# Optimization experiments

Measured on AMD Instinct MI355X. Metric: run time of the kernel, lower is better.

Reference implementation:

```python
import jax, jax.numpy as jnp
import numpy as np

C_S = 384; C_Z = 128; C_RES = 128; H = 12; HD = 32; L = 8; RB = 2; NA = 7
TSF = 10.0; EPS = 1e-8; B = 2; N = 512; NRES = 21


def layernorm(x, g, b, eps=1e-5):
    m = jnp.mean(x, -1, keepdims=True)
    v = jnp.mean((x - m) ** 2, -1, keepdims=True)
    return (x - m) * jax.lax.rsqrt(v + eps) * g + b


def lin(x, w, b=None):
    y = x @ w.T
    return y if b is None else y + b


def rot_vec(R, v):
    return jnp.einsum('...ij,...j->...i', R, v)


def make_rigid(n, ca, c, eps=1e-7):
    # Gram-Schmidt backbone frame construction (openfold make_transform_from_reference)
    t = -ca
    n_xyz = n + t; c_xyz = c + t
    cx, cy, cz = c_xyz[..., 0], c_xyz[..., 1], c_xyz[..., 2]
    z = jnp.zeros_like(cx); o = jnp.ones_like(cx)
    nrm = jnp.sqrt(eps + cx**2 + cy**2)
    s1 = -cy / nrm; c1 = cx / nrm
    R1 = jnp.stack([jnp.stack([c1, -s1, z], -1), jnp.stack([s1, c1, z], -1), jnp.stack([z, z, o], -1)], -2)
    nrm2 = jnp.sqrt(eps + cx**2 + cy**2 + cz**2)
    s2 = cz / nrm2; c2 = jnp.sqrt(cx**2 + cy**2) / nrm2
    R2 = jnp.stack([jnp.stack([c2, z, s2], -1), jnp.stack([z, o, z], -1), jnp.stack([-s2, z, c2], -1)], -2)
    Rc = R2 @ R1
    n2 = rot_vec(Rc, n_xyz)
    ny, nz = n2[..., 1], n2[..., 2]
    nrm3 = jnp.sqrt(eps + ny**2 + nz**2)
    sn = -nz / nrm3; cn = ny / nrm3
    Rn = jnp.stack([jnp.stack([o, z, z], -1), jnp.stack([z, cn, -sn], -1), jnp.stack([z, sn, cn], -1)], -2)
    R = jnp.swapaxes(Rn @ Rc, -1, -2)
    return R, ca


def to4x4(R, t):
    bot = jnp.zeros(R.shape[:-2] + (1, 4), R.dtype).at[..., 0, 3].set(1.0)
    top = jnp.concatenate([R, t[..., None]], -1)
    return jnp.concatenate([top, bot], -2)


def compose(R1, t1, R2, t2):
    return R1 @ R2, rot_vec(R1, t2) + t1


def structure_fwd(s, z, aatype, mask, ln_s_g, ln_s_b, ln_z_g, ln_z_b, w_in, b_in, w_b, b_b,
                  attn_ln_g, attn_ln_b, attn_wqkv, attn_wo, attn_bo, attn_wg, attn_bg,
                  tr_ln_g, tr_ln_b, tr_w1, tr_b1, tr_w2, tr_b2, w_bb, b_bb,
                  ar_win, ar_bin, ar_winit, ar_binit, ar_w1, ar_b1, ar_w2, ar_b2, ar_wout, ar_bout,
                  default_frames, group_idx, atom_mask, lit_positions):
    Bd, Nd = s.shape[:2]
    s = layernorm(s, ln_s_g, ln_s_b)
    s_init = s
    s = lin(s, w_in, b_in)
    zn = layernorm(z, ln_z_g, ln_z_b)
    bmat = lin(zn, w_b, b_b)                                # [B,N,N,L*H]
    bmat = jnp.transpose(bmat, (0, 3, 1, 2)).reshape(Bd, L, H, Nd, Nd)
    key_mask = (mask[:, None, None, :] == 0)
    for i in range(L):
        xn = layernorm(s, attn_ln_g[i], attn_ln_b[i])
        t = lin(xn, attn_wqkv[i]).reshape(Bd, Nd, H, 3 * HD).transpose(0, 2, 1, 3)
        q, k, v = jnp.split(t, 3, axis=-1)                  # each [B,H,N,HD]
        a = jnp.einsum('bhqc,bhkc->bhqk', q * HD ** -0.5, k) + bmat[:, i]
        a = jnp.where(key_mask, -1e9, a)
        a = jax.nn.softmax(a, axis=-1)
        y = jnp.einsum('bhqk,bhkc->bqhc', a, v).reshape(Bd, Nd, C_S)
        g = jax.nn.sigmoid(lin(xn, attn_wg[i], attn_bg[i]))
        s = s + lin(g * y, attn_wo[i], attn_bo[i])
        xt = layernorm(s, tr_ln_g[i], tr_ln_b[i])
        s = s + lin(jax.nn.relu(lin(xt, tr_w1[i], tr_b1[i])), tr_w2[i], tr_b2[i])
    # angle resnet
    a0 = lin(jax.nn.relu(s_init), ar_winit, ar_binit)
    a = lin(jax.nn.relu(s), ar_win, ar_bin) + a0
    for j in range(RB):
        h = lin(jax.nn.relu(a), ar_w1[j], ar_b1[j])
        h = lin(jax.nn.relu(h), ar_w2[j], ar_b2[j])
        a = a + h
    ang = lin(jax.nn.relu(a), ar_wout, ar_bout).reshape(Bd, Nd, NA, 2)
    unnorm = ang
    denom = jnp.sqrt(jnp.maximum(jnp.sum(ang ** 2, -1, keepdims=True), EPS))
    angles = ang / denom
    # backbone rigid from predicted pseudo-atoms
    n_, ca_, c_ = jnp.split(lin(s, w_bb, b_bb), 3, axis=-1)
    Rbb, tbb = make_rigid(n_, ca_, c_)
    tbb = tbb * TSF
    # torsion_angles_to_frames
    d4 = default_frames[aatype]                             # [B,N,8,4,4]
    dR = d4[..., :3, :3]; dt = d4[..., :3, 3]
    bb_sin = jnp.zeros(angles.shape[:-2] + (1,), angles.dtype)
    bb_cos = jnp.ones_like(bb_sin)
    sin_a = jnp.concatenate([bb_sin, angles[..., 0]], -1)   # [B,N,8]
    cos_a = jnp.concatenate([bb_cos, angles[..., 1]], -1)
    z8 = jnp.zeros_like(sin_a); o8 = jnp.ones_like(sin_a)
    Ra = jnp.stack([jnp.stack([o8, z8, z8], -1), jnp.stack([z8, cos_a, -sin_a], -1), jnp.stack([z8, sin_a, cos_a], -1)], -2)
    Rf = dR @ Ra; tf = dt
    R5, t5 = compose(Rf[..., 4, :, :], tf[..., 4, :], Rf[..., 5, :, :], tf[..., 5, :])
    R6, t6 = compose(R5, t5, Rf[..., 6, :, :], tf[..., 6, :])
    R7, t7 = compose(R6, t6, Rf[..., 7, :, :], tf[..., 7, :])
    Rall = jnp.concatenate([Rf[..., :5, :, :], jnp.stack([R5, R6, R7], -3)], -3)
    tall = jnp.concatenate([tf[..., :5, :], jnp.stack([t5, t6, t7], -2)], -2)
    Rg = jnp.einsum('bnij,bngjk->bngik', Rbb, Rall)
    tg = jnp.einsum('bnij,bngj->bngi', Rbb, tall) + tbb[..., None, :]
    # frames + literature positions -> atom14
    oh = jax.nn.one_hot(group_idx[aatype], 8, dtype=Rg.dtype)   # [B,N,14,8]
    Ratom = jnp.einsum('bnag,bngij->bnaij', oh, Rg)
    tatom = jnp.einsum('bnag,bngi->bnai', oh, tg)
    lit = lit_positions[aatype]                             # [B,N,14,3]
    pred = jnp.einsum('bnaij,bnaj->bnai', Ratom, lit) + tatom
    pred = pred * atom_mask[aatype][..., None]
    return angles, unnorm, to4x4(Rbb, tbb), to4x4(Rg, tg), pred, s


def setup_inputs():
    key = jax.random.key(0)
    ks = iter(jax.random.split(key, 64))
    nrm = lambda shape: jax.random.normal(next(ks), shape, jnp.float32) * 0.02
    d = {}
    d['s'] = jax.random.normal(next(ks), (B, N, C_S), jnp.float32)
    d['z'] = jax.random.normal(next(ks), (B, N, N, C_Z), jnp.float32)
    d['aatype'] = jax.random.randint(next(ks), (B, N), 0, NRES)
    d['mask'] = jax.random.randint(next(ks), (B, N), 0, 2).astype(jnp.int32)
    d['ln_s_g'] = jnp.ones(C_S); d['ln_s_b'] = jnp.zeros(C_S)
    d['ln_z_g'] = jnp.ones(C_Z); d['ln_z_b'] = jnp.zeros(C_Z)
    d['w_in'] = nrm((C_S, C_S)); d['b_in'] = jnp.zeros(C_S)
    d['w_b'] = nrm((L * H, C_Z)); d['b_b'] = jnp.zeros(L * H)
    d['attn_ln_g'] = jnp.ones((L, C_S)); d['attn_ln_b'] = jnp.zeros((L, C_S))
    d['attn_wqkv'] = nrm((L, 3 * C_S, C_S))
    d['attn_wo'] = nrm((L, C_S, C_S)); d['attn_bo'] = jnp.zeros((L, C_S))
    d['attn_wg'] = nrm((L, C_S, C_S)); d['attn_bg'] = jnp.ones((L, C_S))
    d['tr_ln_g'] = jnp.ones((L, C_S)); d['tr_ln_b'] = jnp.zeros((L, C_S))
    d['tr_w1'] = nrm((L, C_S, C_S)); d['tr_b1'] = jnp.zeros((L, C_S))
    d['tr_w2'] = nrm((L, C_S, C_S)); d['tr_b2'] = jnp.zeros((L, C_S))
    d['w_bb'] = nrm((9, C_S)); d['b_bb'] = jnp.zeros(9)
    d['ar_win'] = nrm((C_RES, C_S)); d['ar_bin'] = jnp.zeros(C_RES)
    d['ar_winit'] = nrm((C_RES, C_S)); d['ar_binit'] = jnp.zeros(C_RES)
    d['ar_w1'] = nrm((RB, C_RES, C_RES)); d['ar_b1'] = jnp.zeros((RB, C_RES))
    d['ar_w2'] = nrm((RB, C_RES, C_RES)); d['ar_b2'] = jnp.zeros((RB, C_RES))
    d['ar_wout'] = nrm((2 * NA, C_RES)); d['ar_bout'] = jnp.zeros(2 * NA)
    df = jnp.tile(jnp.eye(4, dtype=jnp.float32), (NRES, 8, 1, 1))
    df = df.at[..., :3, 3].set(jax.random.normal(next(ks), (NRES, 8, 3)))
    d['default_frames'] = df
    d['group_idx'] = jax.random.randint(next(ks), (NRES, 14), 0, 8)
    d['atom_mask'] = (jax.random.uniform(next(ks), (NRES, 14)) < 0.9).astype(jnp.float32)
    d['lit_positions'] = jax.random.normal(next(ks), (NRES, 14, 3), jnp.float32)
    return d


def reference(s, z, aatype, mask, ln_s_g, ln_s_b, ln_z_g, ln_z_b, w_in, b_in, w_b, b_b,
              attn_ln_g, attn_ln_b, attn_wqkv, attn_wo, attn_bo, attn_wg, attn_bg,
              tr_ln_g, tr_ln_b, tr_w1, tr_b1, tr_w2, tr_b2, w_bb, b_bb,
              ar_win, ar_bin, ar_winit, ar_binit, ar_w1, ar_b1, ar_w2, ar_b2, ar_wout, ar_bout,
              default_frames, group_idx, atom_mask, lit_positions):
    return structure_fwd(s, z, aatype, mask, ln_s_g, ln_s_b, ln_z_g, ln_z_b, w_in, b_in, w_b, b_b,
                         attn_ln_g, attn_ln_b, attn_wqkv, attn_wo, attn_bo, attn_wg, attn_bg,
                         tr_ln_g, tr_ln_b, tr_w1, tr_b1, tr_w2, tr_b2, w_bb, b_bb,
                         ar_win, ar_bin, ar_winit, ar_binit, ar_w1, ar_b1, ar_w2, ar_b2, ar_wout, ar_bout,
                         default_frames, group_idx, atom_mask, lit_positions)
```

## Files before the change

kernel.cpp:

```cpp
#include <hip/hip_runtime.h>
#include <hip/hip_bf16.h>

typedef __attribute__((ext_vector_type(8))) short bf16x8;
typedef __attribute__((ext_vector_type(4))) float f32x4;
typedef unsigned short u16;

__device__ __forceinline__ u16 f2bf(float f) {
  union { __hip_bfloat16 b; u16 u; } v;
  v.b = __float2bfloat16(f);
  return v.u;
}
__device__ __forceinline__ float bf2f(u16 s) {
  union { unsigned u; float f; } v; v.u = ((unsigned)s) << 16;
  return v.f;
}
__device__ __forceinline__ f32x4 mfma_bf16(bf16x8 a, bf16x8 b, f32x4 c) {
  return __builtin_amdgcn_mfma_f32_16x16x32_bf16(a, b, c, 0, 0, 0);
}
__device__ __forceinline__ void split2(float x, u16& h, u16& l) {
  h = f2bf(x);
  l = f2bf(x - bf2f(h));
}
template <int SPL>
__device__ __forceinline__ void splitN(float x, u16* o) {
  float r = x;
  #pragma unroll
  for (int i = 0; i < SPL; i++) {
    o[i] = f2bf(r);
    if (i + 1 < SPL) r = r - bf2f(o[i]);
  }
}

struct P2 { const float* s; u16* d; int n; };
struct Prep2Args { P2 j[7]; };
__global__ __launch_bounds__(256) void prep2_kernel(Prep2Args A, int total4) {
  for (int i4 = blockIdx.x * 256 + threadIdx.x; i4 < total4; i4 += gridDim.x * 256) {
    int i = i4 * 4;
    #pragma unroll
    for (int jj = 0; jj < 7; jj++) {
      if (i < A.j[jj].n) {
        const float* src = A.j[jj].s;
        u16* dh = A.j[jj].d;
        u16* dl = dh + A.j[jj].n;
        float4 v = *(const float4*)(src + i);
        ushort4 h, l;
        split2(v.x, h.x, l.x); split2(v.y, h.y, l.y);
        split2(v.z, h.z, l.z); split2(v.w, h.w, l.w);
        *(ushort4*)(dh + i) = h;
        *(ushort4*)(dl + i) = l;
        break;
      }
      i -= A.j[jj].n;
    }
  }
}
struct P3 { const float* s; u16* d; int n; };
struct Prep3Args { P3 j[4]; };
__global__ __launch_bounds__(256) void prep3_kernel(Prep3Args A, int total4) {
  for (int i4 = blockIdx.x * 256 + threadIdx.x; i4 < total4; i4 += gridDim.x * 256) {
    int i = i4 * 4;
    #pragma unroll
    for (int jj = 0; jj < 4; jj++) {
      if (i < A.j[jj].n) {
        const float* src = A.j[jj].s;
        u16* d0 = A.j[jj].d;
        u16* d1 = d0 + A.j[jj].n;
        u16* d2 = d1 + A.j[jj].n;
        float4 v = *(const float4*)(src + i);
        float xv[4] = {v.x, v.y, v.z, v.w};
        ushort4 o0, o1, o2;
        u16* po0 = (u16*)&o0; u16* po1 = (u16*)&o1; u16* po2 = (u16*)&o2;
        #pragma unroll
        for (int e = 0; e < 4; e++) {
          u16 tmp[3]; splitN<3>(xv[e], tmp);
          po0[e] = tmp[0]; po1[e] = tmp[1]; po2[e] = tmp[2];
        }
        *(ushort4*)(d0 + i) = o0;
        *(ushort4*)(d1 + i) = o1;
        *(ushort4*)(d2 + i) = o2;
        break;
      }
      i -= A.j[jj].n;
    }
  }
}

__global__ __launch_bounds__(256) void ln_kernel(
    const float* __restrict__ x, const float* __restrict__ gamma,
    const float* __restrict__ beta, float* __restrict__ o, int rows, int C) {
  int wid = threadIdx.x >> 6, lane = threadIdx.x & 63;
  int row = blockIdx.x * 4 + wid;
  if (row >= rows) return;
  const float* xr = x + (size_t)row * C;
  float s = 0.f, s2 = 0.f;
  for (int c = lane; c < C; c += 64) { float v = xr[c]; s += v; s2 += v * v; }
  #pragma unroll
  for (int off = 32; off >= 1; off >>= 1) {
    s += __shfl_xor(s, off);
    s2 += __shfl_xor(s2, off);
  }
  float m = s / C;
  float var = s2 / C - m * m;
  float rs = rsqrtf(var + 1e-5f);
  float* orow = o + (size_t)row * C;
  for (int c = lane; c < C; c += 64) orow[c] = (xr[c] - m) * rs * gamma[c] + beta[c];
}

template <int SPL, int LNA, int INRELU, int ACT, int ACC, int STATS, int OUT2>
__global__ __launch_bounds__(128) void gemm_kernel(
    const float* __restrict__ A, const float* __restrict__ pin,
    const float* __restrict__ lng, const float* __restrict__ lnb,
    const u16* __restrict__ w0p, const u16* __restrict__ w1p, const u16* __restrict__ w2p,
    const float* __restrict__ bias,
    float* __restrict__ O, float* __restrict__ O2, float* __restrict__ pout,
    int M, int N, int K) {
  __shared__ __align__(16) u16 a_pl[SPL][32][72];
  __shared__ __align__(16) u16 w_pl[SPL][32][72];
  const int n0 = blockIdx.x * 32, m0 = blockIdx.y * 32;
  const int t = threadIdx.x;
  const int wid = t >> 6, lane = t & 63;
  const int cl = lane & 15, cg = lane >> 4;
  const int ar = t >> 2, aq = t & 3;
  const float* ap = A + (size_t)(m0 + ar) * K + aq * 16;
  const u16* wp[3] = {nullptr, nullptr, nullptr};
  {
    const u16* tmp[3] = {w0p, w1p, w2p};
    #pragma unroll
    for (int p = 0; p < SPL; p++) wp[p] = tmp[p] + (size_t)(n0 + ar) * K + aq * 16;
  }
  float rm = 0.f, rrs = 1.f;
  if (LNA) {
    float s = 0.f, s2 = 0.f;
    #pragma unroll
    for (int pq = 0; pq < 24; pq++) {
      s  += pin[(m0 + ar) * 48 + pq * 2];
      s2 += pin[(m0 + ar) * 48 + pq * 2 + 1];
    }
    rm = s * (1.f / 384.f);
    rrs = rsqrtf(s2 * (1.f / 384.f) - rm * rm + 1e-5f);
  }
  float4 ra[4], rg[4], rb4[4];
  uint4 rw[SPL][2];
  auto GLOAD = [&](int k0) {
    #pragma unroll
    for (int e = 0; e < 4; e++) ra[e] = ((const float4*)(ap + k0))[e];
    #pragma unroll
    for (int p = 0; p < SPL; p++) {
      rw[p][0] = *(const uint4*)(wp[p] + k0);
      rw[p][1] = *(const uint4*)(wp[p] + k0 + 8);
    }
    if (LNA) {
      #pragma unroll
      for (int e = 0; e < 4; e++) {
        rg[e]  = ((const float4*)(lng + k0 + aq * 16))[e];
        rb4[e] = ((const float4*)(lnb + k0 + aq * 16))[e];
      }
    }
  };
  GLOAD(0);
  f32x4 acc[2] = {};
  for (int k0 = 0; k0 < K; k0 += 64) {
    {
      float av[16];
      #pragma unroll
      for (int e = 0; e < 4; e++) {
        av[e * 4 + 0] = ra[e].x; av[e * 4 + 1] = ra[e].y;
        av[e * 4 + 2] = ra[e].z; av[e * 4 + 3] = ra[e].w;
      }
      if (LNA) {
        #pragma unroll
        for (int e = 0; e < 4; e++) {
          av[e * 4 + 0] = (av[e * 4 + 0] - rm) * rrs * rg[e].x + rb4[e].x;
          av[e * 4 + 1] = (av[e * 4 + 1] - rm) * rrs * rg[e].y + rb4[e].y;
          av[e * 4 + 2] = (av[e * 4 + 2] - rm) * rrs * rg[e].z + rb4[e].z;
          av[e * 4 + 3] = (av[e * 4 + 3] - rm) * rrs * rg[e].w + rb4[e].w;
        }
      }
      if (INRELU) {
        #pragma unroll
        for (int j = 0; j < 16; j++) av[j] = fmaxf(av[j], 0.f);
      }
      u16 sh[SPL][16];
      #pragma unroll
      for (int j = 0; j < 16; j++) {
        u16 tmp[SPL]; splitN<SPL>(av[j], tmp);
        #pragma unroll
        for (int p = 0; p < SPL; p++) sh[p][j] = tmp[p];
      }
      #pragma unroll
      for (int p = 0; p < SPL; p++) {
        *(uint4*)&a_pl[p][ar][aq * 16]     = *(const uint4*)&sh[p][0];
        *(uint4*)&a_pl[p][ar][aq * 16 + 8] = *(const uint4*)&sh[p][8];
        *(uint4*)&w_pl[p][ar][aq * 16]     = rw[p][0];
        *(uint4*)&w_pl[p][ar][aq * 16 + 8] = rw[p][1];
      }
    }
    __syncthreads();
    if (k0 + 64 < K) GLOAD(k0 + 64);
    #pragma unroll
    for (int ks2 = 0; ks2 < 2; ks2++) {
      bf16x8 av_[3][2];
      #pragma unroll
      for (int p = 0; p < SPL; p++) {
        av_[p][0] = *(const bf16x8*)&a_pl[p][cl][ks2 * 32 + cg * 8];
        av_[p][1] = *(const bf16x8*)&a_pl[p][16 + cl][ks2 * 32 + cg * 8];
      }
      bf16x8 bv[3];
      #pragma unroll
      for (int p = 0; p < SPL; p++)
        bv[p] = *(const bf16x8*)&w_pl[p][wid * 16 + cl][ks2 * 32 + cg * 8];
      #pragma unroll
      for (int d = 0; d < SPL; d++)
        #pragma unroll
        for (int i2 = 0; i2 <= d; i2++) {
          acc[0] = mfma_bf16(av_[i2][0], bv[d - i2], acc[0]);
          acc[1] = mfma_bf16(av_[i2][1], bv[d - i2], acc[1]);
        }
    }
    __syncthreads();
  }
  float ps[2][4], ps2[2][4];
  #pragma unroll
  for (int mf = 0; mf < 2; mf++)
    #pragma unroll
    for (int i = 0; i < 4; i++) { ps[mf][i] = 0.f; ps2[mf][i] = 0.f; }
  #pragma unroll
  for (int mf = 0; mf < 2; mf++) {
    #pragma unroll
    for (int i = 0; i < 4; i++) {
      int r = m0 + mf * 16 + cg * 4 + i;
      int c = n0 + wid * 16 + cl;
      float v = acc[mf][i];
      if (bias) v += bias[c];
      if (ACT == 1) v = fmaxf(v, 0.f);
      size_t oi = (size_t)r * N + c;
      float nv = ACC ? (O[oi] + v) : v;
      O[oi] = nv;
      if (OUT2) O2[oi] = nv;
      if (STATS) { ps[mf][i] += nv; ps2[mf][i] += nv * nv; }
    }
  }
  if (STATS) {
    #pragma unroll
    for (int mf = 0; mf < 2; mf++)
      #pragma unroll
      for (int i = 0; i < 4; i++) {
        #pragma unroll
        for (int off = 1; off < 16; off <<= 1) {
          ps[mf][i] += __shfl_xor(ps[mf][i], off);
          ps2[mf][i] += __shfl_xor(ps2[mf][i], off);
        }
      }
    if (cl == 0) {
      #pragma unroll
      for (int mf = 0; mf < 2; mf++)
        #pragma unroll
        for (int i = 0; i < 4; i++) {
          int r = m0 + mf * 16 + cg * 4 + i;
          pout[r * 48 + (blockIdx.x * 2 + wid) * 2] = ps[mf][i];
          pout[r * 48 + (blockIdx.x * 2 + wid) * 2 + 1] = ps2[mf][i];
        }
    }
  }
}

__global__ __launch_bounds__(128) void gemm_qkvg_kernel(
    const float* __restrict__ A, const float* __restrict__ pin,
    const float* __restrict__ lng, const float* __restrict__ lnb,
    const u16* __restrict__ wqh, const u16* __restrict__ wql,
    const u16* __restrict__ wgh, const u16* __restrict__ wgl,
    const float* __restrict__ bg,
    u16* __restrict__ qkvh, u16* __restrict__ qkvl, float* __restrict__ gbuf) {
  __shared__ __align__(16) u16 a_pl[2][32][72];
  __shared__ __align__(16) u16 w_pl[2][32][72];
  const int n0 = blockIdx.x * 32, m0 = blockIdx.y * 32;
  const bool isg = (n0 >= 1152);
  const int t = threadIdx.x;
  const int wid = t >> 6, lane = t & 63;
  const int cl = lane & 15, cg = lane >> 4;
  const int ar = t >> 2, aq = t & 3;
  const float* ap = A + (size_t)(m0 + ar) * 384 + aq * 16;
  const u16* wp0 = (isg ? wgh + (size_t)(n0 - 1152 + ar) * 384 : wqh + (size_t)(n0 + ar) * 384) + aq * 16;
  const u16* wp1 = (isg ? wgl + (size_t)(n0 - 1152 + ar) * 384 : wql + (size_t)(n0 + ar) * 384) + aq * 16;
  float s = 0.f, s2 = 0.f;
  #pragma unroll
  for (int pq = 0; pq < 24; pq++) {
    s  += pin[(m0 + ar) * 48 + pq * 2];
    s2 += pin[(m0 + ar) * 48 + pq * 2 + 1];
  }
  const float rm = s * (1.f / 384.f);
  const float rrs = rsqrtf(s2 * (1.f / 384.f) - rm * rm + 1e-5f);
  float4 ra[4], rg[4], rb4[4];
  uint4 rw0[2], rw1[2];
  auto GLOAD = [&](int k0) {
    #pragma unroll
    for (int e = 0; e < 4; e++) {
      ra[e]  = ((const float4*)(ap + k0))[e];
      rg[e]  = ((const float4*)(lng + k0 + aq * 16))[e];
      rb4[e] = ((const float4*)(lnb + k0 + aq * 16))[e];
    }
    rw0[0] = *(const uint4*)(wp0 + k0);
    rw0[1] = *(const uint4*)(wp0 + k0 + 8);
    rw1[0] = *(const uint4*)(wp1 + k0);
    rw1[1] = *(const uint4*)(wp1 + k0 + 8);
  };
  GLOAD(0);
  f32x4 acc[2] = {};
  for (int k0 = 0; k0 < 384; k0 += 64) {
    {
      float av[16];
      #pragma unroll
      for (int e = 0; e < 4; e++) {
        av[e * 4 + 0] = (ra[e].x - rm) * rrs * rg[e].x + rb4[e].x;
        av[e * 4 + 1] = (ra[e].y - rm) * rrs * rg[e].y + rb4[e].y;
        av[e * 4 + 2] = (ra[e].z - rm) * rrs * rg[e].z + rb4[e].z;
        av[e * 4 + 3] = (ra[e].w - rm) * rrs * rg[e].w + rb4[e].w;
      }
      u16 sh0[16], sh1[16];
      #pragma unroll
      for (int j = 0; j < 16; j++) split2(av[j], sh0[j], sh1[j]);
      *(uint4*)&a_pl[0][ar][aq * 16]     = *(const uint4*)&sh0[0];
      *(uint4*)&a_pl[0][ar][aq * 16 + 8] = *(const uint4*)&sh0[8];
      *(uint4*)&a_pl[1][ar][aq * 16]     = *(const uint4*)&sh1[0];
      *(uint4*)&a_pl[1][ar][aq * 16 + 8] = *(const uint4*)&sh1[8];
      *(uint4*)&w_pl[0][ar][aq * 16]     = rw0[0];
      *(uint4*)&w_pl[0][ar][aq * 16 + 8] = rw0[1];
      *(uint4*)&w_pl[1][ar][aq * 16]     = rw1[0];
      *(uint4*)&w_pl[1][ar][aq * 16 + 8] = rw1[1];
    }
    __syncthreads();
    if (k0 + 64 < 384) GLOAD(k0 + 64);
    #pragma unroll
    for (int ks2 = 0; ks2 < 2; ks2++) {
      bf16x8 ah0 = *(const bf16x8*)&a_pl[0][cl][ks2 * 32 + cg * 8];
      bf16x8 ah1 = *(const bf16x8*)&a_pl[0][16 + cl][ks2 * 32 + cg * 8];
      bf16x8 al0 = *(const bf16x8*)&a_pl[1][cl][ks2 * 32 + cg * 8];
      bf16x8 al1 = *(const bf16x8*)&a_pl[1][16 + cl][ks2 * 32 + cg * 8];
      bf16x8 bh = *(const bf16x8*)&w_pl[0][wid * 16 + cl][ks2 * 32 + cg * 8];
      bf16x8 bl = *(const bf16x8*)&w_pl[1][wid * 16 + cl][ks2 * 32 + cg * 8];
      acc[0] = mfma_bf16(ah0, bh, acc[0]);
      acc[1] = mfma_bf16(ah1, bh, acc[1]);
      acc[0] = mfma_bf16(ah0, bl, acc[0]);
      acc[1] = mfma_bf16(ah1, bl, acc[1]);
      acc[0] = mfma_bf16(al0, bh, acc[0]);
      acc[1] = mfma_bf16(al1, bh, acc[1]);
    }
    __syncthreads();
  }
  #pragma unroll
  for (int mf = 0; mf < 2; mf++) {
    #pragma unroll
    for (int i = 0; i < 4; i++) {
      int r = m0 + mf * 16 + cg * 4 + i;
      int c = n0 + wid * 16 + cl;
      float v = acc[mf][i];
      if (isg) {
        int cc = c - 1152;
        v = 1.f / (1.f + __expf(-(v + bg[cc])));
        gbuf[(size_t)r * 384 + cc] = v;
      } else {
        u16 hh, ll; split2(v, hh, ll);
        qkvh[(size_t)r * 1152 + c] = hh;
        qkvl[(size_t)r * 1152 + c] = ll;
      }
    }
  }
}

__global__ __launch_bounds__(512) void zbmat_kernel(
    const float* __restrict__ z, const float* __restrict__ gamma,
    const float* __restrict__ beta, const u16* __restrict__ wbh,
    const u16* __restrict__ wbl, const float* __restrict__ bbias,
    float* __restrict__ bm) {
  __shared__ __align__(16) u16 w_h[96][136], w_l[96][136];
  __shared__ __align__(16) u16 a_h[2][64][136], a_l[2][64][136];
  const int b = blockIdx.x >> 9, i = blockIdx.x & 511;
  const int t = threadIdx.x;
  for (int idx = t; idx < 1536; idx += 512) {
    int r2 = idx >> 4, c2 = (idx & 15) * 8;
    *(uint4*)&w_h[r2][c2] = *(const uint4*)(wbh + r2 * 128 + c2);
    *(uint4*)&w_l[r2][c2] = *(const uint4*)(wbl + r2 * 128 + c2);
  }
  const int r = t >> 3, q = t & 7;
  const int cq = q * 16;
  const float* zbase = z + ((size_t)(b * 512 + i) * 512) * 128 + (size_t)r * 128 + cq;
  float4 gv[4], bv[4];
  #pragma unroll
  for (int ii = 0; ii < 4; ii++) {
    gv[ii] = *(const float4*)(gamma + cq + ii * 4);
    bv[ii] = *(const float4*)(beta + cq + ii * 4);
  }
  const int wid = t >> 6, lane = t & 63;
  const int cl = lane & 15, cg = lane >> 4;
  const int m = wid & 3, g = wid >> 2;
  const int arow = m * 16 + cl;
  float bb[3];
  #pragma unroll
  for (int nt = 0; nt < 3; nt++) bb[nt] = bbias[(g * 3 + nt) * 16 + cl];
  float4 v[4];

  auto ln_store = [&](int dst) {
    float s = 0.f, s2 = 0.f;
    #pragma unroll
    for (int ii = 0; ii < 4; ii++) {
      s += v[ii].x + v[ii].y + v[ii].z + v[ii].w;
      s2 += v[ii].x * v[ii].x + v[ii].y * v[ii].y + v[ii].z * v[ii].z + v[ii].w * v[ii].w;
    }
    s += __shfl_xor(s, 1); s2 += __shfl_xor(s2, 1);
    s += __shfl_xor(s, 2); s2 += __shfl_xor(s2, 2);
    s += __shfl_xor(s, 4); s2 += __shfl_xor(s2, 4);
    const float mu = s * (1.f / 128.f);
    const float var = s2 * (1.f / 128.f) - mu * mu;
    const float rs = rsqrtf(var + 1e-5f);
    float xv[16];
    #pragma unroll
    for (int w2 = 0; w2 < 4; w2++) {
      float4 x = v[w2], g2 = gv[w2], be = bv[w2];
      xv[w2 * 4 + 0] = (x.x - mu) * rs * g2.x + be.x;
      xv[w2 * 4 + 1] = (x.y - mu) * rs * g2.y + be.y;
      xv[w2 * 4 + 2] = (x.z - mu) * rs * g2.z + be.z;
      xv[w2 * 4 + 3] = (x.w - mu) * rs * g2.w + be.w;
    }
    union { u16 s[8]; uint4 u; } ph, pl;
    #pragma unroll
    for (int j = 0; j < 8; j++) split2(xv[j], ph.s[j], pl.s[j]);
    *(uint4*)&a_h[dst][r][cq] = ph.u;
    *(uint4*)&a_l[dst][r][cq] = pl.u;
    #pragma unroll
    for (int j = 0; j < 8; j++) split2(xv[8 + j], ph.s[j], pl.s[j]);
    *(uint4*)&a_h[dst][r][cq + 8] = ph.u;
    *(uint4*)&a_l[dst][r][cq + 8] = pl.u;
  };

  #pragma unroll
  for (int ii = 0; ii < 4; ii++) v[ii] = ((const float4*)zbase)[ii];
  ln_store(0);
  __syncthreads();

  int cur = 0;
  for (int jt = 0; jt < 8; jt++) {
    if (jt < 7) {
      const float* src = zbase + (size_t)(jt + 1) * 64 * 128;
      #pragma unroll
      for (int ii = 0; ii < 4; ii++) v[ii] = ((const float4*)src)[ii];
    }
    f32x4 acc[3] = {};
    #pragma unroll
    for (int ks = 0; ks < 4; ks++) {
      bf16x8 ah = *(const bf16x8*)&a_h[cur][arow][ks * 32 + cg * 8];
      bf16x8 al = *(const bf16x8*)&a_l[cur][arow][ks * 32 + cg * 8];
      bf16x8 bh[3], bl[3];
      #pragma unroll
      for (int nt = 0; nt < 3; nt++) {
        bh[nt] = *(const bf16x8*)&w_h[(g * 3 + nt) * 16 + cl][ks * 32 + cg * 8];
        bl[nt] = *(const bf16x8*)&w_l[(g * 3 + nt) * 16 + cl][ks * 32 + cg * 8];
      }
      #pragma unroll
      for (int nt = 0; nt < 3; nt++) acc[nt] = mfma_bf16(ah, bh[nt], acc[nt]);
      #pragma unroll
      for (int nt = 0; nt < 3; nt++) acc[nt] = mfma_bf16(ah, bl[nt], acc[nt]);
      #pragma unroll
      for (int nt = 0; nt < 3; nt++) acc[nt] = mfma_bf16(al, bh[nt], acc[nt]);
    }
    #pragma unroll
    for (int nt = 0; nt < 3; nt++) {
      float4 o;
      o.x = acc[nt][0] + bb[nt]; o.y = acc[nt][1] + bb[nt];
      o.z = acc[nt][2] + bb[nt]; o.w = acc[nt][3] + bb[nt];
      int ch = (g * 3 + nt) * 16 + cl;
      *(float4*)&bm[((size_t)(b * 96 + ch) * 512 + i) * 512 + jt * 64 + m * 16 + cg * 4] = o;
    }
    if (jt < 7) ln_store(cur ^ 1);
    __syncthreads();
    cur ^= 1;
  }
}

__global__ __launch_bounds__(128) void attn_kernel(
    const u16* __restrict__ qkvh, const u16* __restrict__ qkvl,
    const float* __restrict__ bmat, const int* __restrict__ maskp,
    const float* __restrict__ gate, float* __restrict__ ybuf, int layer) {
  __shared__ __align__(16) u16 vT_h[32][522];
  __shared__ __align__(16) u16 vT_l[32][522];
  __shared__ __align__(16) u16 pst_h[2][16][36];
  __shared__ __align__(16) u16 pst_l[2][16][36];
  const int bid = blockIdx.x;
  const int qb = bid & 15;
  const int hh = (bid >> 4) % 12;
  const int b = bid / 192;
  const int q0 = qb * 32;
  const int t = threadIdx.x;
  const int wid = t >> 6;
  const int lane = t & 63;
  const int cl = lane & 15, cg = lane >> 4;

  for (int idx = t; idx < 2048; idx += 128) {
    int k = idx >> 2, c8 = (idx & 3) * 8;
    size_t off = (size_t)(b * 512 + k) * 1152 + hh * 96 + 64 + c8;
    union { uint4 u; u16 s[8]; } vh, vl;
    vh.u = *(const uint4*)(qkvh + off);
    vl.u = *(const uint4*)(qkvl + off);
    #pragma unroll
    for (int j = 0; j < 8; j++) {
      vT_h[c8 + j][k] = vh.s[j];
      vT_l[c8 + j][k] = vl.s[j];
    }
  }

  const int qrow = q0 + wid * 16 + cl;
  const size_t qoff = (size_t)(b * 512 + qrow) * 1152 + hh * 96 + cg * 8;
  bf16x8 qh = *(const bf16x8*)(qkvh + qoff);
  bf16x8 ql = *(const bf16x8*)(qkvl + qoff);

  __syncthreads();

  const f32x4 zero4 = {0.f, 0.f, 0.f, 0.f};
  const float qs = 0.17677669529663687f;
  f32x4 sc[32];
  #pragma unroll
  for (int nt = 0; nt < 32; nt++) {
    int kk = nt * 16 + cl;
    size_t koff = (size_t)(b * 512 + kk) * 1152 + hh * 96 + 32 + cg * 8;
    bf16x8 kh = *(const bf16x8*)(qkvh + koff);
    bf16x8 kl = *(const bf16x8*)(qkvl + koff);
    f32x4 a = mfma_bf16(qh, kh, zero4);
    a = mfma_bf16(qh, kl, a);
    a = mfma_bf16(ql, kh, a);
    sc[nt] = a;
  }

  const size_t bc = (size_t)(b * 96 + layer * 12 + hh);
  #pragma unroll
  for (int nt = 0; nt < 32; nt++) {
    int kk = nt * 16 + cl;
    int mk = maskp[b * 512 + kk];
    #pragma unroll
    for (int i2 = 0; i2 < 4; i2++) {
      int qq = q0 + wid * 16 + cg * 4 + i2;
      float bias = bmat[(bc * 512 + qq) * 512 + kk];
      float vv = sc[nt][i2] * qs + bias;
      sc[nt][i2] = (mk == 0) ? -1e9f : vv;
    }
  }

  float inv[4];
  #pragma unroll
  for (int i2 = 0; i2 < 4; i2++) {
    float mx = -3e38f;
    #pragma unroll
    for (int nt = 0; nt < 32; nt++) mx = fmaxf(mx, sc[nt][i2]);
    mx = fmaxf(mx, __shfl_xor(mx, 1));
    mx = fmaxf(mx, __shfl_xor(mx, 2));
    mx = fmaxf(mx, __shfl_xor(mx, 4));
    mx = fmaxf(mx, __shfl_xor(mx, 8));
    float ss = 0.f;
    #pragma unroll
    for (int nt = 0; nt < 32; nt++) {
      float p = __expf(sc[nt][i2] - mx);
      sc[nt][i2] = p;
      ss += p;
    }
    ss += __shfl_xor(ss, 1);
    ss += __shfl_xor(ss, 2);
    ss += __shfl_xor(ss, 4);
    ss += __shfl_xor(ss, 8);
    inv[i2] = 1.f / ss;
  }

  f32x4 yacc[2] = {};
  for (int ks = 0; ks < 16; ks++) {
    #pragma unroll
    for (int half = 0; half < 2; half++) {
      int nt = ks * 2 + half;
      #pragma unroll
      for (int i2 = 0; i2 < 4; i2++) {
        u16 h2, l2; split2(sc[nt][i2] * inv[i2], h2, l2);
        pst_h[wid][cg * 4 + i2][half * 16 + cl] = h2;
        pst_l[wid][cg * 4 + i2][half * 16 + cl] = l2;
      }
    }
    __syncthreads();
    bf16x8 ph = *(const bf16x8*)&pst_h[wid][cl][cg * 8];
    bf16x8 pl = *(const bf16x8*)&pst_l[wid][cl][cg * 8];
    #pragma unroll
    for (int nt2 = 0; nt2 < 2; nt2++) {
      bf16x8 vh = *(const bf16x8*)&vT_h[nt2 * 16 + cl][ks * 32 + cg * 8];
      bf16x8 vl = *(const bf16x8*)&vT_l[nt2 * 16 + cl][ks * 32 + cg * 8];
      yacc[nt2] = mfma_bf16(ph, vh, yacc[nt2]);
      yacc[nt2] = mfma_bf16(ph, vl, yacc[nt2]);
      yacc[nt2] = mfma_bf16(pl, vh, yacc[nt2]);
    }
    __syncthreads();
  }

  #pragma unroll
  for (int nt2 = 0; nt2 < 2; nt2++) {
    #pragma unroll
    for (int i2 = 0; i2 < 4; i2++) {
      int qq = q0 + wid * 16 + cg * 4 + i2;
      int c = nt2 * 16 + cl;
      size_t oi = (size_t)(b * 512 + qq) * 384 + hh * 32 + c;
      ybuf[oi] = yacc[nt2][i2] * gate[oi];
    }
  }
}

template <int NOUT, int K, int RELU>
__global__ __launch_bounds__(256) void proj_kernel(
    const float* __restrict__ A, const float* __restrict__ W,
    const float* __restrict__ bias, float* __restrict__ O) {
  const int wid = threadIdx.x >> 6, lane = threadIdx.x & 63;
  const int row = blockIdx.x * 4 + wid;
  const float* a = A + (size_t)row * K;
  float av[K / 64];
  #pragma unroll
  for (int j = 0; j < K / 64; j++) {
    float v = a[lane + 64 * j];
    av[j] = RELU ? fmaxf(v, 0.f) : v;
  }
  float res = 0.f;
  #pragma unroll
  for (int n = 0; n < NOUT; n++) {
    float s = 0.f;
    #pragma unroll
    for (int j = 0; j < K / 64; j++) s += av[j] * W[n * K + lane + 64 * j];
    #pragma unroll
    for (int off = 32; off >= 1; off >>= 1) s += __shfl_xor(s, off);
    if (lane == n) res = s + bias[n];
  }
  if (lane < NOUT) O[(size_t)row * NOUT + lane] = res;
}

__device__ __forceinline__ void m3m(float* o, const float* a, const float* b) {
  #pragma unroll
  for (int i = 0; i < 3; i++)
    #pragma unroll
    for (int j = 0; j < 3; j++)
      o[i * 3 + j] = a[i * 3 + 0] * b[0 * 3 + j] + a[i * 3 + 1] * b[1 * 3 + j] + a[i * 3 + 2] * b[2 * 3 + j];
}
__device__ __forceinline__ void m3v(float* o, const float* a, const float* v) {
  #pragma unroll
  for (int i = 0; i < 3; i++)
    o[i] = a[i * 3 + 0] * v[0] + a[i * 3 + 1] * v[1] + a[i * 3 + 2] * v[2];
}

__global__ __launch_bounds__(256) void tail_kernel(
    const float* __restrict__ angraw, const float* __restrict__ bbbuf,
    const int* __restrict__ aatype, const float* __restrict__ deff,
    const int* __restrict__ gidx, const float* __restrict__ amask,
    const float* __restrict__ lit,
    float* __restrict__ o_ang, float* __restrict__ o_un,
    float* __restrict__ o_bb4, float* __restrict__ o_rg4, float* __restrict__ o_pred) {
  int idx = blockIdx.x * 256 + threadIdx.x;
  if (idx >= 1024) return;
  float ang[14];
  #pragma unroll
  for (int a = 0; a < 7; a++) {
    float s0 = angraw[idx * 14 + a * 2], s1 = angraw[idx * 14 + a * 2 + 1];
    o_un[(idx * 7 + a) * 2] = s0; o_un[(idx * 7 + a) * 2 + 1] = s1;
    float d = sqrtf(fmaxf(s0 * s0 + s1 * s1, 1e-8f));
    ang[a * 2] = s0 / d; ang[a * 2 + 1] = s1 / d;
    o_ang[(idx * 7 + a) * 2] = ang[a * 2]; o_ang[(idx * 7 + a) * 2 + 1] = ang[a * 2 + 1];
  }
  const float* p = bbbuf + (size_t)idx * 9;
  float nx = p[0] - p[3], ny = p[1] - p[4], nz = p[2] - p[5];
  float cx = p[6] - p[3], cy = p[7] - p[4], cz = p[8] - p[5];
  const float eps = 1e-7f;
  float nrm = sqrtf(eps + cx * cx + cy * cy);
  float s1 = -cy / nrm, c1 = cx / nrm;
  float nrm2 = sqrtf(eps + cx * cx + cy * cy + cz * cz);
  float s2 = cz / nrm2, c2 = sqrtf(cx * cx + cy * cy) / nrm2;
  float Rc[9] = { c2 * c1, -c2 * s1, s2,
                  s1,      c1,       0.f,
                  -s2 * c1, s2 * s1, c2 };
  float n2y = Rc[3] * nx + Rc[4] * ny + Rc[5] * nz;
  float n2z = Rc[6] * nx + Rc[7] * ny + Rc[8] * nz;
  float nrm3 = sqrtf(eps + n2y * n2y + n2z * n2z);
  float sn = -n2z / nrm3, cn = n2y / nrm3;
  float Rm[9];
  Rm[0] = Rc[0]; Rm[1] = Rc[1]; Rm[2] = Rc[2];
  Rm[3] = cn * Rc[3] - sn * Rc[6];
  Rm[4] = cn * Rc[4] - sn * Rc[7];
  Rm[5] = cn * Rc[5] - sn * Rc[8];
  Rm[6] = sn * Rc[3] + cn * Rc[6];
  Rm[7] = sn * Rc[4] + cn * Rc[7];
  Rm[8] = sn * Rc[5] + cn * Rc[8];
  float Rb[9] = { Rm[0], Rm[3], Rm[6],
                  Rm[1], Rm[4], Rm[7],
                  Rm[2], Rm[5], Rm[8] };
  float tb[3] = { p[3] * 10.f, p[4] * 10.f, p[5] * 10.f };
  {
    float* o = o_bb4 + (size_t)idx * 16;
    o[0] = Rb[0]; o[1] = Rb[1]; o[2] = Rb[2]; o[3] = tb[0];
    o[4] = Rb[3]; o[5] = Rb[4]; o[6] = Rb[5]; o[7] = tb[1];
    o[8] = Rb[6]; o[9] = Rb[7]; o[10] = Rb[8]; o[11] = tb[2];
    o[12] = 0.f; o[13] = 0.f; o[14] = 0.f; o[15] = 1.f;
  }
  int aa = aatype[idx];
  float Rf[8][9], tf[8][3];
  for (int g = 0; g < 8; g++) {
    const float* d4 = deff + ((size_t)aa * 8 + g) * 16;
    float sa = 0.f, ca = 1.f;
    if (g > 0) { sa = ang[(g - 1) * 2]; ca = ang[(g - 1) * 2 + 1]; }
    #pragma unroll
    for (int i = 0; i < 3; i++) {
      float d0 = d4[i * 4 + 0], d1 = d4[i * 4 + 1], d2 = d4[i * 4 + 2];
      Rf[g][i * 3 + 0] = d0;
      Rf[g][i * 3 + 1] = d1 * ca + d2 * sa;
      Rf[g][i * 3 + 2] = -d1 * sa + d2 * ca;
      tf[g][i] = d4[i * 4 + 3];
    }
  }
  float Rall[8][9], tall[8][3];
  for (int g = 0; g < 5; g++) {
    #pragma unroll
    for (int i = 0; i < 9; i++) Rall[g][i] = Rf[g][i];
    #pragma unroll
    for (int i = 0; i < 3; i++) tall[g][i] = tf[g][i];
  }
  m3m(Rall[5], Rf[4], Rf[5]); m3v(tall[5], Rf[4], tf[5]);
  tall[5][0] += tf[4][0]; tall[5][1] += tf[4][1]; tall[5][2] += tf[4][2];
  m3m(Rall[6], Rall[5], Rf[6]); m3v(tall[6], Rall[5], tf[6]);
  tall[6][0] += tall[5][0]; tall[6][1] += tall[5][1]; tall[6][2] += tall[5][2];
  m3m(Rall[7], Rall[6], Rf[7]); m3v(tall[7], Rall[6], tf[7]);
  tall[7][0] += tall[6][0]; tall[7][1] += tall[6][1]; tall[7][2] += tall[6][2];
  float RG[8][9], TG[8][3];
  for (int g = 0; g < 8; g++) {
    m3m(RG[g], Rb, Rall[g]);
    m3v(TG[g], Rb, tall[g]);
    TG[g][0] += tb[0]; TG[g][1] += tb[1]; TG[g][2] += tb[2];
    float* o = o_rg4 + ((size_t)idx * 8 + g) * 16;
    o[0] = RG[g][0]; o[1] = RG[g][1]; o[2] = RG[g][2]; o[3] = TG[g][0];
    o[4] = RG[g][3]; o[5] = RG[g][4]; o[6] = RG[g][5]; o[7] = TG[g][1];
    o[8] = RG[g][6]; o[9] = RG[g][7]; o[10] = RG[g][8]; o[11] = TG[g][2];
    o[12] = 0.f; o[13] = 0.f; o[14] = 0.f; o[15] = 1.f;
  }
  for (int a = 0; a < 14; a++) {
    int gi = gidx[aa * 14 + a];
    const float* lp = lit + ((size_t)aa * 14 + a) * 3;
    float mk = amask[aa * 14 + a];
    float px = RG[gi][0] * lp[0] + RG[gi][1] * lp[1] + RG[gi][2] * lp[2] + TG[gi][0];
    float py = RG[gi][3] * lp[0] + RG[gi][4] * lp[1] + RG[gi][5] * lp[2] + TG[gi][1];
    float pz = RG[gi][6] * lp[0] + RG[gi][7] * lp[1] + RG[gi][8] * lp[2] + TG[gi][2];
    float* op = o_pred + ((size_t)idx * 14 + a) * 3;
    op[0] = px * mk; op[1] = py * mk; op[2] = pz * mk;
  }
}

extern "C" void kernel_launch(void* const* d_in, const int* in_sizes, int n_in,
                              void* d_out, int out_size, void* d_ws, size_t ws_size,
                              hipStream_t stream) {
  (void)in_sizes; (void)n_in; (void)out_size; (void)ws_size;
  const float* s_in    = (const float*)d_in[0];
  const float* z_in    = (const float*)d_in[1];
  const int*   aatype  = (const int*)d_in[2];
  const int*   maskp   = (const int*)d_in[3];
  const float* ln_s_g  = (const float*)d_in[4];
  const float* ln_s_b  = (const float*)d_in[5];
  const float* ln_z_g  = (const float*)d_in[6];
  const float* ln_z_b  = (const float*)d_in[7];
  const float* w_in    = (const float*)d_in[8];
  const float* b_in    = (const float*)d_in[9];
  const float* w_b     = (const float*)d_in[10];
  const float* b_b     = (const float*)d_in[11];
  const float* attn_ln_g = (const float*)d_in[12];
  const float* attn_ln_b = (const float*)d_in[13];
  const float* attn_wqkv = (const float*)d_in[14];
  const float* attn_wo   = (const float*)d_in[15];
  const float* attn_bo   = (const float*)d_in[16];
  const float* attn_wg   = (const float*)d_in[17];
  const float* attn_bg   = (const float*)d_in[18];
  const float* tr_ln_g   = (const float*)d_in[19];
  const float* tr_ln_b   = (const float*)d_in[20];
  const float* tr_w1     = (const float*)d_in[21];
  const float* tr_b1     = (const float*)d_in[22];
  const float* tr_w2     = (const float*)d_in[23];
  const float* tr_b2     = (const float*)d_in[24];
  const float* w_bb      = (const float*)d_in[25];
  const float* b_bb      = (const float*)d_in[26];
  const float* ar_win    = (const float*)d_in[27];
  const float* ar_bin    = (const float*)d_in[28];
  const float* ar_winit  = (const float*)d_in[29];
  const float* ar_binit  = (const float*)d_in[30];
  const float* ar_w1     = (const float*)d_in[31];
  const float* ar_b1     = (const float*)d_in[32];
  const float* ar_w2     = (const float*)d_in[33];
  const float* ar_b2     = (const float*)d_in[34];
  const float* ar_wout   = (const float*)d_in[35];
  const float* ar_bout   = (const float*)d_in[36];
  const float* def_frames= (const float*)d_in[37];
  const int*   group_idx = (const int*)d_in[38];
  const float* atom_mask = (const float*)d_in[39];
  const float* lit_pos   = (const float*)d_in[40];

  char* p = (char*)d_ws;
  float* bmat   = (float*)p;          p += 201326592;
  float* s_init = (float*)p;          p += 1572864;
  float* s_cur  = (float*)p;          p += 1572864;
  u16*   qkvh   = (u16*)p;            p += 2359296;
  u16*   qkvl   = (u16*)p;            p += 2359296;
  float* gbuf   = (float*)p;          p += 1572864;
  float* ybuf   = (float*)p;          p += 1572864;
  float* h1buf  = (float*)p;          p += 1572864;
  float* abuf   = (float*)p;          p += 524288;
  float* htmp   = (float*)p;          p += 524288;
  float* pbuf   = (float*)p;          p += 196608;
  float* bbbuf  = (float*)p;          p += 65536;
  float* angraw = (float*)p;          p += 57344;
  u16* ps_qkvw  = (u16*)p;            p += 14155776;
  u16* ps_wg    = (u16*)p;            p += 4718592;
  u16* ps_wo    = (u16*)p;            p += 4718592;
  u16* ps_tr1   = (u16*)p;            p += 4718592;
  u16* ps_tr2   = (u16*)p;            p += 4718592;
  u16* ps_win   = (u16*)p;            p += 589824;
  u16* ps_wb    = (u16*)p;            p += 49152;
  u16* ps_arwin = (u16*)p;            p += 294912;
  u16* ps_arwinit = (u16*)p;          p += 294912;
  u16* ps_arw1  = (u16*)p;            p += 196608;
  u16* ps_arw2  = (u16*)p;            p += 196608;

  float* out    = (float*)d_out;
  float* o_ang  = out;
  float* o_un   = out + 14336;
  float* o_bb4  = out + 28672;
  float* o_rg4  = out + 45056;
  float* o_pred = out + 176128;
  float* o_s    = out + 219136;

  Prep2Args p2;
  p2.j[0] = {attn_wqkv, ps_qkvw, 3538944};
  p2.j[1] = {attn_wg,   ps_wg,   1179648};
  p2.j[2] = {attn_wo,   ps_wo,   1179648};
  p2.j[3] = {tr_w1,     ps_tr1,  1179648};
  p2.j[4] = {tr_w2,     ps_tr2,  1179648};
  p2.j[5] = {w_in,      ps_win,  147456};
  p2.j[6] = {w_b,       ps_wb,   12288};
  prep2_kernel<<<2048, 256, 0, stream>>>(p2, 2104320);
  Prep3Args p3;
  p3.j[0] = {ar_win,   ps_arwin,   49152};
  p3.j[1] = {ar_winit, ps_arwinit, 49152};
  p3.j[2] = {ar_w1,    ps_arw1,    32768};
  p3.j[3] = {ar_w2,    ps_arw2,    32768};
  prep3_kernel<<<160, 256, 0, stream>>>(p3, 40960);

  ln_kernel<<<256, 256, 0, stream>>>(s_in, ln_s_g, ln_s_b, s_init, 1024, 384);
  gemm_kernel<2, 0, 0, 0, 0, 1, 0><<<dim3(12, 32), 128, 0, stream>>>(
      s_init, nullptr, nullptr, nullptr, ps_win, ps_win + 147456, nullptr,
      b_in, s_cur, nullptr, pbuf, 1024, 384, 384);
  zbmat_kernel<<<1024, 512, 0, stream>>>(z_in, ln_z_g, ln_z_b, ps_wb, ps_wb + 12288, b_b, bmat);

  for (int l = 0; l < 8; ++l) {
    gemm_qkvg_kernel<<<dim3(48, 32), 128, 0, stream>>>(
        s_cur, pbuf, attn_ln_g + l * 384, attn_ln_b + l * 384,
        ps_qkvw + (size_t)l * 442368, ps_qkvw + 3538944 + (size_t)l * 442368,
        ps_wg + (size_t)l * 147456, ps_wg + 1179648 + (size_t)l * 147456,
        attn_bg + l * 384, qkvh, qkvl, gbuf);
    attn_kernel<<<384, 128, 0, stream>>>(qkvh, qkvl, bmat, maskp, gbuf, ybuf, l);
    gemm_kernel<2, 0, 0, 0, 1, 1, 0><<<dim3(12, 32), 128, 0, stream>>>(
        ybuf, nullptr, nullptr, nullptr,
        ps_wo + (size_t)l * 147456, ps_wo + 1179648 + (size_t)l * 147456, nullptr,
        attn_bo + l * 384, s_cur, nullptr, pbuf, 1024, 384, 384);
    gemm_kernel<2, 1, 0, 1, 0, 0, 0><<<dim3(12, 32), 128, 0, stream>>>(
        s_cur, pbuf, tr_ln_g + l * 384, tr_ln_b + l * 384,
        ps_tr1 + (size_t)l * 147456, ps_tr1 + 1179648 + (size_t)l * 147456, nullptr,
        tr_b1 + l * 384, h1buf, nullptr, nullptr, 1024, 384, 384);
    if (l < 7)
      gemm_kernel<2, 0, 0, 0, 1, 1, 0><<<dim3(12, 32), 128, 0, stream>>>(
          h1buf, nullptr, nullptr, nullptr,
          ps_tr2 + (size_t)l * 147456, ps_tr2 + 1179648 + (size_t)l * 147456, nullptr,
          tr_b2 + l * 384, s_cur, nullptr, pbuf, 1024, 384, 384);
    else
      gemm_kernel<2, 0, 0, 0, 1, 1, 1><<<dim3(12, 32), 128, 0, stream>>>(
          h1buf, nullptr, nullptr, nullptr,
          ps_tr2 + (size_t)l * 147456, ps_tr2 + 1179648 + (size_t)l * 147456, nullptr,
          tr_b2 + l * 384, s_cur, o_s, pbuf, 1024, 384, 384);
  }

  gemm_kernel<3, 0, 1, 0, 0, 0, 0><<<dim3(4, 32), 128, 0, stream>>>(
      s_cur, nullptr, nullptr, nullptr,
      ps_arwin, ps_arwin + 49152, ps_arwin + 98304,
      ar_bin, abuf, nullptr, nullptr, 1024, 128, 384);
  gemm_kernel<3, 0, 1, 0, 1, 0, 0><<<dim3(4, 32), 128, 0, stream>>>(
      s_init, nullptr, nullptr, nullptr,
      ps_arwinit, ps_arwinit + 49152, ps_arwinit + 98304,
      ar_binit, abuf, nullptr, nullptr, 1024, 128, 384);
  for (int j = 0; j < 2; ++j) {
    gemm_kernel<3, 0, 1, 0, 0, 0, 0><<<dim3(4, 32), 128, 0, stream>>>(
        abuf, nullptr, nullptr, nullptr,
        ps_arw1 + j * 16384, ps_arw1 + 32768 + j * 16384, ps_arw1 + 65536 + j * 16384,
        ar_b1 + j * 128, htmp, nullptr, nullptr, 1024, 128, 128);
    gemm_kernel<3, 0, 1, 0, 1, 0, 0><<<dim3(4, 32), 128, 0, stream>>>(
        htmp, nullptr, nullptr, nullptr,
        ps_arw2 + j * 16384, ps_arw2 + 32768 + j * 16384, ps_arw2 + 65536 + j * 16384,
        ar_b2 + j * 128, abuf, nullptr, nullptr, 1024, 128, 128);
  }

  proj_kernel<9, 384, 0><<<256, 256, 0, stream>>>(s_cur, w_bb, b_bb, bbbuf);
  proj_kernel<14, 128, 1><<<256, 256, 0, stream>>>(abuf, ar_wout, ar_bout, angraw);
  tail_kernel<<<4, 256, 0, stream>>>(angraw, bbbuf, aatype, def_frames, group_idx,
                                     atom_mask, lit_pos, o_ang, o_un, o_bb4, o_rg4, o_pred);
}
```

Before: 1.157 ms.

## Fuse transformer layer loop into persistent kernel with software grid barriers

Replaces the 40 per-layer launches (qkvg gemm, attention, out-proj, two transition gemms) with a single persistent kernel of 384 blocks. Phases are separated by an atomic-counter grid barrier. GEMM tiles are widened from 32x32 to 32x64, so each wave computes four N-tiles and reuses its A fragment, and the layernorm partial-stats buffer shrinks to match. This removes launch and inter-kernel drain overhead, but relies on all 384 blocks being co-resident without a cooperative launch, and the barrier has a bounded spin guard.

New measurement: 2.796 ms. 2.42x slower.

```diff
diff --git a/kernel.cpp b/kernel.cpp
--- a/kernel.cpp
+++ b/kernel.cpp
@@ -29,6 +29,23 @@
     o[i] = f2bf(r);
     if (i + 1 < SPL) r = r - bf2f(o[i]);
   }
+}
+
+__device__ __forceinline__ void gsync(unsigned* cnt, int nb, int* gen) {
+  __syncthreads();
+  if (threadIdx.x == 0) {
+    __threadfence();
+    *gen += 1;
+    atomicAdd(cnt, 1u);
+    const unsigned target = (unsigned)nb * (unsigned)(*gen);
+    int guard = 0;
+    while (atomicAdd(cnt, 0u) < target && guard < (1 << 26)) {
+      __builtin_amdgcn_s_sleep(8);
+      guard++;
+    }
+    __threadfence();
+  }
+  __syncthreads();
 }
 
 struct P2 { const float* s; u16* d; int n; };
@@ -115,40 +132,40 @@
     float* __restrict__ O, float* __restrict__ O2, float* __restrict__ pout,
     int M, int N, int K) {
   __shared__ __align__(16) u16 a_pl[SPL][32][72];
-  __shared__ __align__(16) u16 w_pl[SPL][32][72];
-  const int n0 = blockIdx.x * 32, m0 = blockIdx.y * 32;
+  __shared__ __align__(16) u16 w_pl[SPL][64][72];
+  const int n0 = blockIdx.x * 64, m0 = blockIdx.y * 32;
   const int t = threadIdx.x;
   const int wid = t >> 6, lane = t & 63;
   const int cl = lane & 15, cg = lane >> 4;
   const int ar = t >> 2, aq = t & 3;
+  const int wr = t >> 1, wh2 = t & 1;
   const float* ap = A + (size_t)(m0 + ar) * K + aq * 16;
   const u16* wp[3] = {nullptr, nullptr, nullptr};
   {
     const u16* tmp[3] = {w0p, w1p, w2p};
     #pragma unroll
-    for (int p = 0; p < SPL; p++) wp[p] = tmp[p] + (size_t)(n0 + ar) * K + aq * 16;
+    for (int p = 0; p < SPL; p++) wp[p] = tmp[p] + (size_t)(n0 + wr) * K + wh2 * 32;
   }
   float rm = 0.f, rrs = 1.f;
   if (LNA) {
     float s = 0.f, s2 = 0.f;
     #pragma unroll
-    for (int pq = 0; pq < 24; pq++) {
-      s  += pin[(m0 + ar) * 48 + pq * 2];
-      s2 += pin[(m0 + ar) * 48 + pq * 2 + 1];
+    for (int pq = 0; pq < 6; pq++) {
+      s  += pin[(m0 + ar) * 16 + pq * 2];
+      s2 += pin[(m0 + ar) * 16 + pq * 2 + 1];
     }
     rm = s * (1.f / 384.f);
     rrs = rsqrtf(s2 * (1.f / 384.f) - rm * rm + 1e-5f);
   }
   float4 ra[4], rg[4], rb4[4];
-  uint4 rw[SPL][2];
+  uint4 rw[SPL][4];
   auto GLOAD = [&](int k0) {
     #pragma unroll
     for (int e = 0; e < 4; e++) ra[e] = ((const float4*)(ap + k0))[e];
     #pragma unroll
-    for (int p = 0; p < SPL; p++) {
-      rw[p][0] = *(const uint4*)(wp[p] + k0);
-      rw[p][1] = *(const uint4*)(wp[p] + k0 + 8);
-    }
+    for (int p = 0; p < SPL; p++)
+      #pragma unroll
+      for (int e = 0; e < 4; e++) rw[p][e] = *(const uint4*)(wp[p] + k0 + e * 8);
     if (LNA) {
       #pragma unroll
       for (int e = 0; e < 4; e++) {
@@ -158,7 +175,7 @@
     }
   };
   GLOAD(0);
-  f32x4 acc[2] = {};
+  f32x4 acc[4] = {};
   for (int k0 = 0; k0 < K; k0 += 64) {
     {
       float av[16];
@@ -191,177 +208,69 @@
       for (int p = 0; p < SPL; p++) {
         *(uint4*)&a_pl[p][ar][aq * 16]     = *(const uint4*)&sh[p][0];
         *(uint4*)&a_pl[p][ar][aq * 16 + 8] = *(const uint4*)&sh[p][8];
-        *(uint4*)&w_pl[p][ar][aq * 16]     = rw[p][0];
-        *(uint4*)&w_pl[p][ar][aq * 16 + 8] = rw[p][1];
+        #pragma unroll
+        for (int e = 0; e < 4; e++) *(uint4*)&w_pl[p][wr][wh2 * 32 + e * 8] = rw[p][e];
       }
     }
     __syncthreads();
     if (k0 + 64 < K) GLOAD(k0 + 64);
     #pragma unroll
     for (int ks2 = 0; ks2 < 2; ks2++) {
-      bf16x8 av_[3][2];
-      #pragma unroll
-      for (int p = 0; p < SPL; p++) {
-        av_[p][0] = *(const bf16x8*)&a_pl[p][cl][ks2 * 32 + cg * 8];
-        av_[p][1] = *(const bf16x8*)&a_pl[p][16 + cl][ks2 * 32 + cg * 8];
-      }
-      bf16x8 bv[3];
+      bf16x8 av_[SPL];
       #pragma unroll
       for (int p = 0; p < SPL; p++)
-        bv[p] = *(const bf16x8*)&w_pl[p][wid * 16 + cl][ks2 * 32 + cg * 8];
+        av_[p] = *(const bf16x8*)&a_pl[p][wid * 16 + cl][ks2 * 32 + cg * 8];
+      bf16x8 bv[SPL][4];
+      #pragma unroll
+      for (int p = 0; p < SPL; p++)
+        #pragma unroll
+        for (int nt = 0; nt < 4; nt++)
+          bv[p][nt] = *(const bf16x8*)&w_pl[p][nt * 16 + cl][ks2 * 32 + cg * 8];
       #pragma unroll
       for (int d = 0; d < SPL; d++)
         #pragma unroll
         for (int i2 = 0; i2 <= d; i2++) {
-          acc[0] = mfma_bf16(av_[i2][0], bv[d - i2], acc[0]);
-          acc[1] = mfma_bf16(av_[i2][1], bv[d - i2], acc[1]);
+          #pragma unroll
+          for (int nt = 0; nt < 4; nt++)
+            acc[nt] = mfma_bf16(av_[i2], bv[d - i2][nt], acc[nt]);
         }
     }
     __syncthreads();
   }
-  float ps[2][4], ps2[2][4];
-  #pragma unroll
-  for (int mf = 0; mf < 2; mf++)
-    #pragma unroll
-    for (int i = 0; i < 4; i++) { ps[mf][i] = 0.f; ps2[mf][i] = 0.f; }
-  #pragma unroll
-  for (int mf = 0; mf < 2; mf++) {
+  float ps[4], ps2[4];
+  #pragma unroll
+  for (int i = 0; i < 4; i++) { ps[i] = 0.f; ps2[i] = 0.f; }
+  #pragma unroll
+  for (int nt = 0; nt < 4; nt++) {
     #pragma unroll
     for (int i = 0; i < 4; i++) {
-      int r = m0 + mf * 16 + cg * 4 + i;
-      int c = n0 + wid * 16 + cl;
-      float v = acc[mf][i];
+      int r = m0 + wid * 16 + cg * 4 + i;
+      int c = n0 + nt * 16 + cl;
+      float v = acc[nt][i];
       if (bias) v += bias[c];
       if (ACT == 1) v = fmaxf(v, 0.f);
       size_t oi = (size_t)r * N + c;
       float nv = ACC ? (O[oi] + v) : v;
       O[oi] = nv;
       if (OUT2) O2[oi] = nv;
-      if (STATS) { ps[mf][i] += nv; ps2[mf][i] += nv * nv; }
+      if (STATS) { ps[i] += nv; ps2[i] += nv * nv; }
     }
   }
   if (STATS) {
     #pragma unroll
-    for (int mf = 0; mf < 2; mf++)
+    for (int i = 0; i < 4; i++) {
+      #pragma unroll
+      for (int off = 1; off < 16; off <<= 1) {
+        ps[i] += __shfl_xor(ps[i], off);
+        ps2[i] += __shfl_xor(ps2[i], off);
+      }
+    }
+    if (cl == 0) {
       #pragma unroll
       for (int i = 0; i < 4; i++) {
-        #pragma unroll
-        for (int off = 1; off < 16; off <<= 1) {
-          ps[mf][i] += __shfl_xor(ps[mf][i], off);
-          ps2[mf][i] += __shfl_xor(ps2[mf][i], off);
-        }
-      }
-    if (cl == 0) {
-      #pragma unroll
-      for (int mf = 0; mf < 2; mf++)
-        #pragma unroll
-        for (int i = 0; i < 4; i++) {
-          int r = m0 + mf * 16 + cg * 4 + i;
-          pout[r * 48 + (blockIdx.x * 2 + wid) * 2] = ps[mf][i];
-          pout[r * 48 + (blockIdx.x * 2 + wid) * 2 + 1] = ps2[mf][i];
-        }
-    }
-  }
-}
-
-__global__ __launch_bounds__(128) void gemm_qkvg_kernel(
-    const float* __restrict__ A, const float* __restrict__ pin,
-    const float* __restrict__ lng, const float* __restrict__ lnb,
-    const u16* __restrict__ wqh, const u16* __restrict__ wql,
-    const u16* __restrict__ wgh, const u16* __restrict__ wgl,
-    const float* __restrict__ bg,
-    u16* __restrict__ qkvh, u16* __restrict__ qkvl, float* __restrict__ gbuf) {
-  __shared__ __align__(16) u16 a_pl[2][32][72];
-  __shared__ __align__(16) u16 w_pl[2][32][72];
-  const int n0 = blockIdx.x * 32, m0 = blockIdx.y * 32;
-  const bool isg = (n0 >= 1152);
-  const int t = threadIdx.x;
-  const int wid = t >> 6, lane = t & 63;
-  const int cl = lane & 15, cg = lane >> 4;
-  const int ar = t >> 2, aq = t & 3;
-  const float* ap = A + (size_t)(m0 + ar) * 384 + aq * 16;
-  const u16* wp0 = (isg ? wgh + (size_t)(n0 - 1152 + ar) * 384 : wqh + (size_t)(n0 + ar) * 384) + aq * 16;
-  const u16* wp1 = (isg ? wgl + (size_t)(n0 - 1152 + ar) * 384 : wql + (size_t)(n0 + ar) * 384) + aq * 16;
-  float s = 0.f, s2 = 0.f;
-  #pragma unroll
-  for (int pq = 0; pq < 24; pq++) {
-    s  += pin[(m0 + ar) * 48 + pq * 2];
-    s2 += pin[(m0 + ar) * 48 + pq * 2 + 1];
-  }
-  const float rm = s * (1.f / 384.f);
-  const float rrs = rsqrtf(s2 * (1.f / 384.f) - rm * rm + 1e-5f);
-  float4 ra[4], rg[4], rb4[4];
-  uint4 rw0[2], rw1[2];
-  auto GLOAD = [&](int k0) {
-    #pragma unroll
-    for (int e = 0; e < 4; e++) {
-      ra[e]  = ((const float4*)(ap + k0))[e];
-      rg[e]  = ((const float4*)(lng + k0 + aq * 16))[e];
-      rb4[e] = ((const float4*)(lnb + k0 + aq * 16))[e];
-    }
-    rw0[0] = *(const uint4*)(wp0 + k0);
-    rw0[1] = *(const uint4*)(wp0 + k0 + 8);
-    rw1[0] = *(const uint4*)(wp1 + k0);
-    rw1[1] = *(const uint4*)(wp1 + k0 + 8);
-  };
-  GLOAD(0);
-  f32x4 acc[2] = {};
-  for (int k0 = 0; k0 < 384; k0 += 64) {
-    {
-      float av[16];
-      #pragma unroll
-      for (int e = 0; e < 4; e++) {
-        av[e * 4 + 0] = (ra[e].x - rm) * rrs * rg[e].x + rb4[e].x;
-        av[e * 4 + 1] = (ra[e].y - rm) * rrs * rg[e].y + rb4[e].y;
-        av[e * 4 + 2] = (ra[e].z - rm) * rrs * rg[e].z + rb4[e].z;
-        av[e * 4 + 3] = (ra[e].w - rm) * rrs * rg[e].w + rb4[e].w;
-      }
-      u16 sh0[16], sh1[16];
-      #pragma unroll
-      for (int j = 0; j < 16; j++) split2(av[j], sh0[j], sh1[j]);
-      *(uint4*)&a_pl[0][ar][aq * 16]     = *(const uint4*)&sh0[0];
-      *(uint4*)&a_pl[0][ar][aq * 16 + 8] = *(const uint4*)&sh0[8];
-      *(uint4*)&a_pl[1][ar][aq * 16]     = *(const uint4*)&sh1[0];
-      *(uint4*)&a_pl[1][ar][aq * 16 + 8] = *(const uint4*)&sh1[8];
-      *(uint4*)&w_pl[0][ar][aq * 16]     = rw0[0];
-      *(uint4*)&w_pl[0][ar][aq * 16 + 8] = rw0[1];
-      *(uint4*)&w_pl[1][ar][aq * 16]     = rw1[0];
-      *(uint4*)&w_pl[1][ar][aq * 16 + 8] = rw1[1];
-    }
-    __syncthreads();
-    if (k0 + 64 < 384) GLOAD(k0 + 64);
-    #pragma unroll
-    for (int ks2 = 0; ks2 < 2; ks2++) {
-      bf16x8 ah0 = *(const bf16x8*)&a_pl[0][cl][ks2 * 32 + cg * 8];
-      bf16x8 ah1 = *(const bf16x8*)&a_pl[0][16 + cl][ks2 * 32 + cg * 8];
-      bf16x8 al0 = *(const bf16x8*)&a_pl[1][cl][ks2 * 32 + cg * 8];
-      bf16x8 al1 = *(const bf16x8*)&a_pl[1][16 + cl][ks2 * 32 + cg * 8];
-      bf16x8 bh = *(const bf16x8*)&w_pl[0][wid * 16 + cl][ks2 * 32 + cg * 8];
-      bf16x8 bl = *(const bf16x8*)&w_pl[1][wid * 16 + cl][ks2 * 32 + cg * 8];
-      acc[0] = mfma_bf16(ah0, bh, acc[0]);
-      acc[1] = mfma_bf16(ah1, bh, acc[1]);
-      acc[0] = mfma_bf16(ah0, bl, acc[0]);
-      acc[1] = mfma_bf16(ah1, bl, acc[1]);
-      acc[0] = mfma_bf16(al0, bh, acc[0]);
-      acc[1] = mfma_bf16(al1, bh, acc[1]);
-    }
-    __syncthreads();
-  }
-  #pragma unroll
-  for (int mf = 0; mf < 2; mf++) {
-    #pragma unroll
-    for (int i = 0; i < 4; i++) {
-      int r = m0 + mf * 16 + cg * 4 + i;
-      int c = n0 + wid * 16 + cl;
-      float v = acc[mf][i];
-      if (isg) {
-        int cc = c - 1152;
-        v = 1.f / (1.f + __expf(-(v + bg[cc])));
-        gbuf[(size_t)r * 384 + cc] = v;
-      } else {
-        u16 hh, ll; split2(v, hh, ll);
-        qkvh[(size_t)r * 1152 + c] = hh;
-        qkvl[(size_t)r * 1152 + c] = ll;
+        int r = m0 + wid * 16 + cg * 4 + i;
+        pout[r * 16 + blockIdx.x * 2] = ps[i];
+        pout[r * 16 + blockIdx.x * 2 + 1] = ps2[i];
       }
     }
   }
@@ -476,18 +385,273 @@
   }
 }
 
-__global__ __launch_bounds__(128) void attn_kernel(
+struct CoopArgs {
+  float* s_cur; float* pbuf;
+  u16* qkvh; u16* qkvl; float* gbuf; float* ybuf; float* h1buf;
+  const float* bmat; const int* maskp;
+  const u16* ps_qkvw; const u16* ps_wg; const u16* ps_wo;
+  const u16* ps_tr1; const u16* ps_tr2;
+  const float* attn_ln_g; const float* attn_ln_b;
+  const float* attn_bg; const float* attn_bo;
+  const float* tr_ln_g; const float* tr_ln_b;
+  const float* tr_b1; const float* tr_b2;
+  float* o_s;
+};
+
+template <int LNA, int ACT, int ACC, int STATS, int OUT2>
+__device__ void gemm_job(char* smem, int m0, int n0,
+    const float* __restrict__ A, const float* __restrict__ pin,
+    const float* __restrict__ lng, const float* __restrict__ lnb,
+    const u16* __restrict__ w0p, const u16* __restrict__ w1p,
+    const float* __restrict__ bias,
+    float* __restrict__ O, float* __restrict__ O2, float* __restrict__ pout,
+    int N, int K) {
+  u16 (*a_pl)[32][72] = (u16 (*)[32][72])smem;
+  u16 (*w_pl)[64][72] = (u16 (*)[64][72])(smem + 9216);
+  const int t = threadIdx.x;
+  const int wid = t >> 6, lane = t & 63;
+  const int cl = lane & 15, cg = lane >> 4;
+  const int ar = t >> 2, aq = t & 3;
+  const int wr = t >> 1, wh2 = t & 1;
+  const float* ap = A + (size_t)(m0 + ar) * K + aq * 16;
+  const u16* wp0 = w0p + (size_t)(n0 + wr) * K + wh2 * 32;
+  const u16* wp1 = w1p + (size_t)(n0 + wr) * K + wh2 * 32;
+  float rm = 0.f, rrs = 1.f;
+  if (LNA) {
+    float s = 0.f, s2 = 0.f;
+    #pragma unroll
+    for (int pq = 0; pq < 6; pq++) {
+      s  += pin[(m0 + ar) * 16 + pq * 2];
+      s2 += pin[(m0 + ar) * 16 + pq * 2 + 1];
+    }
+    rm = s * (1.f / 384.f);
+    rrs = rsqrtf(s2 * (1.f / 384.f) - rm * rm + 1e-5f);
+  }
+  float4 ra[4], rg[4], rb4[4];
+  uint4 rw0[4], rw1[4];
+  auto GLOAD = [&](int k0) {
+    #pragma unroll
+    for (int e = 0; e < 4; e++) {
+      ra[e]  = ((const float4*)(ap + k0))[e];
+      rw0[e] = *(const uint4*)(wp0 + k0 + e * 8);
+      rw1[e] = *(const uint4*)(wp1 + k0 + e * 8);
+    }
+    if (LNA) {
+      #pragma unroll
+      for (int e = 0; e < 4; e++) {
+        rg[e]  = ((const float4*)(lng + k0 + aq * 16))[e];
+        rb4[e] = ((const float4*)(lnb + k0 + aq * 16))[e];
+      }
+    }
+  };
+  GLOAD(0);
+  f32x4 acc[4] = {};
+  for (int k0 = 0; k0 < K; k0 += 64) {
+    {
+      float av[16];
+      #pragma unroll
+      for (int e = 0; e < 4; e++) {
+        av[e * 4 + 0] = ra[e].x; av[e * 4 + 1] = ra[e].y;
+        av[e * 4 + 2] = ra[e].z; av[e * 4 + 3] = ra[e].w;
+      }
+      if (LNA) {
+        #pragma unroll
+        for (int e = 0; e < 4; e++) {
+          av[e * 4 + 0] = (av[e * 4 + 0] - rm) * rrs * rg[e].x + rb4[e].x;
+          av[e * 4 + 1] = (av[e * 4 + 1] - rm) * rrs * rg[e].y + rb4[e].y;
+          av[e * 4 + 2] = (av[e * 4 + 2] - rm) * rrs * rg[e].z + rb4[e].z;
+          av[e * 4 + 3] = (av[e * 4 + 3] - rm) * rrs * rg[e].w + rb4[e].w;
+        }
+      }
+      u16 sh0[16], sh1[16];
+      #pragma unroll
+      for (int j = 0; j < 16; j++) split2(av[j], sh0[j], sh1[j]);
+      *(uint4*)&a_pl[0][ar][aq * 16]     = *(const uint4*)&sh0[0];
+      *(uint4*)&a_pl[0][ar][aq * 16 + 8] = *(const uint4*)&sh0[8];
+      *(uint4*)&a_pl[1][ar][aq * 16]     = *(const uint4*)&sh1[0];
+      *(uint4*)&a_pl[1][ar][aq * 16 + 8] = *(const uint4*)&sh1[8];
+      #pragma unroll
+      for (int e = 0; e < 4; e++) {
+        *(uint4*)&w_pl[0][wr][wh2 * 32 + e * 8] = rw0[e];
+        *(uint4*)&w_pl[1][wr][wh2 * 32 + e * 8] = rw1[e];
+      }
+    }
+    __syncthreads();
+    if (k0 + 64 < K) GLOAD(k0 + 64);
+    #pragma unroll
+    for (int ks2 = 0; ks2 < 2; ks2++) {
+      bf16x8 ah = *(const bf16x8*)&a_pl[0][wid * 16 + cl][ks2 * 32 + cg * 8];
+      bf16x8 al = *(const bf16x8*)&a_pl[1][wid * 16 + cl][ks2 * 32 + cg * 8];
+      bf16x8 bh[4], bl[4];
+      #pragma unroll
+      for (int nt = 0; nt < 4; nt++) {
+        bh[nt] = *(const bf16x8*)&w_pl[0][nt * 16 + cl][ks2 * 32 + cg * 8];
+        bl[nt] = *(const bf16x8*)&w_pl[1][nt * 16 + cl][ks2 * 32 + cg * 8];
+      }
+      #pragma unroll
+      for (int nt = 0; nt < 4; nt++) acc[nt] = mfma_bf16(ah, bh[nt], acc[nt]);
+      #pragma unroll
+      for (int nt = 0; nt < 4; nt++) acc[nt] = mfma_bf16(ah, bl[nt], acc[nt]);
+      #pragma unroll
+      for (int nt = 0; nt < 4; nt++) acc[nt] = mfma_bf16(al, bh[nt], acc[nt]);
+    }
+    __syncthreads();
+  }
+  float ps[4], ps2[4];
+  #pragma unroll
+  for (int i = 0; i < 4; i++) { ps[i] = 0.f; ps2[i] = 0.f; }
+  #pragma unroll
+  for (int nt = 0; nt < 4; nt++) {
+    #pragma unroll
+    for (int i = 0; i < 4; i++) {
+      int r = m0 + wid * 16 + cg * 4 + i;
+      int c = n0 + nt * 16 + cl;
+      float v = acc[nt][i];
+      v += bias[c];
+      if (ACT == 1) v = fmaxf(v, 0.f);
+      size_t oi = (size_t)r * N + c;
+      float nv = ACC ? (O[oi] + v) : v;
+      O[oi] = nv;
+      if (OUT2) O2[oi] = nv;
+      if (STATS) { ps[i] += nv; ps2[i] += nv * nv; }
+    }
+  }
+  if (STATS) {
+    #pragma unroll
+    for (int i = 0; i < 4; i++) {
+      #pragma unroll
+      for (int off = 1; off < 16; off <<= 1) {
+        ps[i] += __shfl_xor(ps[i], off);
+        ps2[i] += __shfl_xor(ps2[i], off);
+      }
+    }
+    if (cl == 0) {
+      int nblk = n0 >> 6;
+      #pragma unroll
+      for (int i = 0; i < 4; i++) {
+        int r = m0 + wid * 16 + cg * 4 + i;
+        pout[r * 16 + nblk * 2] = ps[i];
+        pout[r * 16 + nblk * 2 + 1] = ps2[i];
+      }
+    }
+  }
+}
+
+__device__ void qkvg_job(char* smem, int m0, int n0,
+    const float* __restrict__ A, const float* __restrict__ pin,
+    const float* __restrict__ lng, const float* __restrict__ lnb,
+    const u16* __restrict__ wqh, const u16* __restrict__ wql,
+    const u16* __restrict__ wgh, const u16* __restrict__ wgl,
+    const float* __restrict__ bg,
+    u16* __restrict__ qkvh, u16* __restrict__ qkvl, float* __restrict__ gbuf) {
+  u16 (*a_pl)[32][72] = (u16 (*)[32][72])smem;
+  u16 (*w_pl)[64][72] = (u16 (*)[64][72])(smem + 9216);
+  const bool isg = (n0 >= 1152);
+  const int t = threadIdx.x;
+  const int wid = t >> 6, lane = t & 63;
+  const int cl = lane & 15, cg = lane >> 4;
+  const int ar = t >> 2, aq = t & 3;
+  const int wr = t >> 1, wh2 = t & 1;
+  const float* ap = A + (size_t)(m0 + ar) * 384 + aq * 16;
+  const u16* wp0 = (isg ? wgh + (size_t)(n0 - 1152 + wr) * 384 : wqh + (size_t)(n0 + wr) * 384) + wh2 * 32;
+  const u16* wp1 = (isg ? wgl + (size_t)(n0 - 1152 + wr) * 384 : wql + (size_t)(n0 + wr) * 384) + wh2 * 32;
+  float s = 0.f, s2 = 0.f;
+  #pragma unroll
+  for (int pq = 0; pq < 6; pq++) {
+    s  += pin[(m0 + ar) * 16 + pq * 2];
+    s2 += pin[(m0 + ar) * 16 + pq * 2 + 1];
+  }
+  const float rm = s * (1.f / 384.f);
+  const float rrs = rsqrtf(s2 * (1.f / 384.f) - rm * rm + 1e-5f);
+  float4 ra[4], rg[4], rb4[4];
+  uint4 rw0[4], rw1[4];
+  auto GLOAD = [&](int k0) {
+    #pragma unroll
+    for (int e = 0; e < 4; e++) {
+      ra[e]  = ((const float4*)(ap + k0))[e];
+      rw0[e] = *(const uint4*)(wp0 + k0 + e * 8);
+      rw1[e] = *(const uint4*)(wp1 + k0 + e * 8);
+      rg[e]  = ((const float4*)(lng + k0 + aq * 16))[e];
+      rb4[e] = ((const float4*)(lnb + k0 + aq * 16))[e];
+    }
+  };
+  GLOAD(0);
+  f32x4 acc[4] = {};
+  for (int k0 = 0; k0 < 384; k0 += 64) {
+    {
+      float av[16];
+      #pragma unroll
+      for (int e = 0; e < 4; e++) {
+        av[e * 4 + 0] = (ra[e].x - rm) * rrs * rg[e].x + rb4[e].x;
+        av[e * 4 + 1] = (ra[e].y - rm) * rrs * rg[e].y + rb4[e].y;
+        av[e * 4 + 2] = (ra[e].z - rm) * rrs * rg[e].z + rb4[e].z;
+        av[e * 4 + 3] = (ra[e].w - rm) * rrs * rg[e].w + rb4[e].w;
+      }
+      u16 sh0[16], sh1[16];
+      #pragma unroll
+      for (int j = 0; j < 16; j++) split2(av[j], sh0[j], sh1[j]);
+      *(uint4*)&a_pl[0][ar][aq * 16]     = *(const uint4*)&sh0[0];
+      *(uint4*)&a_pl[0][ar][aq * 16 + 8] = *(const uint4*)&sh0[8];
+      *(uint4*)&a_pl[1][ar][aq * 16]     = *(const uint4*)&sh1[0];
+      *(uint4*)&a_pl[1][ar][aq * 16 + 8] = *(const uint4*)&sh1[8];
+      #pragma unroll
+      for (int e = 0; e < 4; e++) {
+        *(uint4*)&w_pl[0][wr][wh2 * 32 + e * 8] = rw0[e];
+        *(uint4*)&w_pl[1][wr][wh2 * 32 + e * 8] = rw1[e];
+      }
+    }
+    __syncthreads();
+    if (k0 + 64 < 384) GLOAD(k0 + 64);
+    #pragma unroll
+    for (int ks2 = 0; ks2 < 2; ks2++) {
+      bf16x8 ah = *(const bf16x8*)&a_pl[0][wid * 16 + cl][ks2 * 32 + cg * 8];
+      bf16x8 al = *(const bf16x8*)&a_pl[1][wid * 16 + cl][ks2 * 32 + cg * 8];
+      bf16x8 bh[4], bl[4];
+      #pragma unroll
+      for (int nt = 0; nt < 4; nt++) {
+        bh[nt] = *(const bf16x8*)&w_pl[0][nt * 16 + cl][ks2 * 32 + cg * 8];
+        bl[nt] = *(const bf16x8*)&w_pl[1][nt * 16 + cl][ks2 * 32 + cg * 8];
+      }
+      #pragma unroll
+      for (int nt = 0; nt < 4; nt++) acc[nt] = mfma_bf16(ah, bh[nt], acc[nt]);
+      #pragma unroll
+      for (int nt = 0; nt < 4; nt++) acc[nt] = mfma_bf16(ah, bl[nt], acc[nt]);
+      #pragma unroll
+      for (int nt = 0; nt < 4; nt++) acc[nt] = mfma_bf16(al, bh[nt], acc[nt]);
+    }
+    __syncthreads();
+  }
+  #pragma unroll
+  for (int nt = 0; nt < 4; nt++) {
+    #pragma unroll
+    for (int i = 0; i < 4; i++) {
+      int r = m0 + wid * 16 + cg * 4 + i;
+      int c = n0 + nt * 16 + cl;
+      float v = acc[nt][i];
+      if (isg) {
+        int cc = c - 1152;
+        v = 1.f / (1.f + __expf(-(v + bg[cc])));
+        gbuf[(size_t)r * 384 + cc] = v;
+      } else {
+        u16 hh, ll; split2(v, hh, ll);
+        qkvh[(size_t)r * 1152 + c] = hh;
+        qkvl[(size_t)r * 1152 + c] = ll;
+      }
+    }
+  }
+}
+
+__device__ void attn_job(char* smem, int job, int layer,
     const u16* __restrict__ qkvh, const u16* __restrict__ qkvl,
     const float* __restrict__ bmat, const int* __restrict__ maskp,
-    const float* __restrict__ gate, float* __restrict__ ybuf, int layer) {
-  __shared__ __align__(16) u16 vT_h[32][522];
-  __shared__ __align__(16) u16 vT_l[32][522];
-  __shared__ __align__(16) u16 pst_h[2][16][36];
-  __shared__ __align__(16) u16 pst_l[2][16][36];
-  const int bid = blockIdx.x;
-  const int qb = bid & 15;
-  const int hh = (bid >> 4) % 12;
-  const int b = bid / 192;
+    const float* __restrict__ gate, float* __restrict__ ybuf) {
+  u16 (*vT_h)[522] = (u16 (*)[522])smem;
+  u16 (*vT_l)[522] = (u16 (*)[522])(smem + 33408);
+  u16 (*pst_h)[16][36] = (u16 (*)[16][36])(smem + 66816);
+  u16 (*pst_l)[16][36] = (u16 (*)[16][36])(smem + 69120);
+  const int qb = job & 15;
+  const int hh = (job >> 4) % 12;
+  const int b = job / 192;
   const int q0 = qb * 32;
   const int t = threadIdx.x;
   const int wid = t >> 6;
@@ -602,6 +766,53 @@
       size_t oi = (size_t)(b * 512 + qq) * 384 + hh * 32 + c;
       ybuf[oi] = yacc[nt2][i2] * gate[oi];
     }
+  }
+}
+
+__global__ __launch_bounds__(128) void layers_kernel(CoopArgs a, unsigned* cnt) {
+  __shared__ __align__(16) char smem[71424];
+  int gen = 0;
+  const int nb = gridDim.x;
+  const int bid = blockIdx.x;
+  for (int l = 0; l < 8; ++l) {
+    const u16* wqh = a.ps_qkvw + (size_t)l * 442368;
+    const u16* wql = a.ps_qkvw + 3538944 + (size_t)l * 442368;
+    const u16* wgh = a.ps_wg + (size_t)l * 147456;
+    const u16* wgl = a.ps_wg + 1179648 + (size_t)l * 147456;
+    for (int j = bid; j < 768; j += nb)
+      qkvg_job(smem, (j / 24) * 32, (j % 24) * 64, a.s_cur, a.pbuf,
+               a.attn_ln_g + l * 384, a.attn_ln_b + l * 384,
+               wqh, wql, wgh, wgl, a.attn_bg + l * 384, a.qkvh, a.qkvl, a.gbuf);
+    gsync(cnt, nb, &gen);
+    for (int j = bid; j < 384; j += nb)
+      attn_job(smem, j, l, a.qkvh, a.qkvl, a.bmat, a.maskp, a.gbuf, a.ybuf);
+    gsync(cnt, nb, &gen);
+    for (int j = bid; j < 192; j += nb)
+      gemm_job<0, 0, 1, 1, 0>(smem, (j / 6) * 32, (j % 6) * 64, a.ybuf,
+          nullptr, nullptr, nullptr,
+          a.ps_wo + (size_t)l * 147456, a.ps_wo + 1179648 + (size_t)l * 147456,
+          a.attn_bo + l * 384, a.s_cur, nullptr, a.pbuf, 384, 384);
+    gsync(cnt, nb, &gen);
+    for (int j = bid; j < 192; j += nb)
+      gemm_job<1, 1, 0, 0, 0>(smem, (j / 6) * 32, (j % 6) * 64, a.s_cur,
+          a.pbuf, a.tr_ln_g + l * 384, a.tr_ln_b + l * 384,
+          a.ps_tr1 + (size_t)l * 147456, a.ps_tr1 + 1179648 + (size_t)l * 147456,
+          a.tr_b1 + l * 384, a.h1buf, nullptr, nullptr, 384, 384);
+    gsync(cnt, nb, &gen);
+    if (l < 7) {
+      for (int j = bid; j < 192; j += nb)
+        gemm_job<0, 0, 1, 1, 0>(smem, (j / 6) * 32, (j % 6) * 64, a.h1buf,
+            nullptr, nullptr, nullptr,
+            a.ps_tr2 + (size_t)l * 147456, a.ps_tr2 + 1179648 + (size_t)l * 147456,
+            a.tr_b2 + l * 384, a.s_cur, nullptr, a.pbuf, 384, 384);
+    } else {
+      for (int j = bid; j < 192; j += nb)
+        gemm_job<0, 0, 1, 1, 1>(smem, (j / 6) * 32, (j % 6) * 64, a.h1buf,
+            nullptr, nullptr, nullptr,
+            a.ps_tr2 + (size_t)l * 147456, a.ps_tr2 + 1179648 + (size_t)l * 147456,
+            a.tr_b2 + l * 384, a.s_cur, a.o_s, a.pbuf, 384, 384);
+    }
+    if (l < 7) gsync(cnt, nb, &gen);
   }
 }
 
@@ -804,9 +1015,10 @@
   float* h1buf  = (float*)p;          p += 1572864;
   float* abuf   = (float*)p;          p += 524288;
   float* htmp   = (float*)p;          p += 524288;
-  float* pbuf   = (float*)p;          p += 196608;
+  float* pbuf   = (float*)p;          p += 131072;
   float* bbbuf  = (float*)p;          p += 65536;
   float* angraw = (float*)p;          p += 57344;
+  unsigned* sync_cnt = (unsigned*)p;  p += 256;
   u16* ps_qkvw  = (u16*)p;            p += 14155776;
   u16* ps_wg    = (u16*)p;            p += 4718592;
   u16* ps_wo    = (u16*)p;            p += 4718592;
@@ -844,52 +1056,40 @@
   prep3_kernel<<<160, 256, 0, stream>>>(p3, 40960);
 
   ln_kernel<<<256, 256, 0, stream>>>(s_in, ln_s_g, ln_s_b, s_init, 1024, 384);
-  gemm_kernel<2, 0, 0, 0, 0, 1, 0><<<dim3(12, 32), 128, 0, stream>>>(
+  gemm_kernel<2, 0, 0, 0, 0, 1, 0><<<dim3(6, 32), 128, 0, stream>>>(
       s_init, nullptr, nullptr, nullptr, ps_win, ps_win + 147456, nullptr,
       b_in, s_cur, nullptr, pbuf, 1024, 384, 384);
   zbmat_kernel<<<1024, 512, 0, stream>>>(z_in, ln_z_g, ln_z_b, ps_wb, ps_wb + 12288, b_b, bmat);
 
-  for (int l = 0; l < 8; ++l) {
-    gemm_qkvg_kernel<<<dim3(48, 32), 128, 0, stream>>>(
-        s_cur, pbuf, attn_ln_g + l * 384, attn_ln_b + l * 384,
-        ps_qkvw + (size_t)l * 442368, ps_qkvw + 3538944 + (size_t)l * 442368,
-        ps_wg + (size_t)l * 147456, ps_wg + 1179648 + (size_t)l * 147456,
-        attn_bg + l * 384, qkvh, qkvl, gbuf);
-    attn_kernel<<<384, 128, 0, stream>>>(qkvh, qkvl, bmat, maskp, gbuf, ybuf, l);
-    gemm_kernel<2, 0, 0, 0, 1, 1, 0><<<dim3(12, 32), 128, 0, stream>>>(
-        ybuf, nullptr, nullptr, nullptr,
-        ps_wo + (size_t)l * 147456, ps_wo + 1179648 + (size_t)l * 147456, nullptr,
-        attn_bo + l * 384, s_cur, nullptr, pbuf, 1024, 384, 384);
-    gemm_kernel<2, 1, 0, 1, 0, 0, 0><<<dim3(12, 32), 128, 0, stream>>>(
-        s_cur, pbuf, tr_ln_g + l * 384, tr_ln_b + l * 384,
-        ps_tr1 + (size_t)l * 147456, ps_tr1 + 1179648 + (size_t)l * 147456, nullptr,
-        tr_b1 + l * 384, h1buf, nullptr, nullptr, 1024, 384, 384);
-    if (l < 7)
-      gemm_kernel<2, 0, 0, 0, 1, 1, 0><<<dim3(12, 32), 128, 0, stream>>>(
-          h1buf, nullptr, nullptr, nullptr,
-          ps_tr2 + (size_t)l * 147456, ps_tr2 + 1179648 + (size_t)l * 147456, nullptr,
-          tr_b2 + l * 384, s_cur, nullptr, pbuf, 1024, 384, 384);
-    else
-      gemm_kernel<2, 0, 0, 0, 1, 1, 1><<<dim3(12, 32), 128, 0, stream>>>(
-          h1buf, nullptr, nullptr, nullptr,
-          ps_tr2 + (size_t)l * 147456, ps_tr2 + 1179648 + (size_t)l * 147456, nullptr,
-          tr_b2 + l * 384, s_cur, o_s, pbuf, 1024, 384, 384);
-  }
-
-  gemm_kernel<3, 0, 1, 0, 0, 0, 0><<<dim3(4, 32), 128, 0, stream>>>(
+  hipError_t mem_err = hipMemsetAsync(sync_cnt, 0, 256, stream);
+  (void)mem_err;
+  CoopArgs ca;
+  ca.s_cur = s_cur; ca.pbuf = pbuf;
+  ca.qkvh = qkvh; ca.qkvl = qkvl; ca.gbuf = gbuf; ca.ybuf = ybuf; ca.h1buf = h1buf;
+  ca.bmat = bmat; ca.maskp = maskp;
+  ca.ps_qkvw = ps_qkvw; ca.ps_wg = ps_wg; ca.ps_wo = ps_wo;
+  ca.ps_tr1 = ps_tr1; ca.ps_tr2 = ps_tr2;
+  ca.attn_ln_g = attn_ln_g; ca.attn_ln_b = attn_ln_b;
+  ca.attn_bg = attn_bg; ca.attn_bo = attn_bo;
+  ca.tr_ln_g = tr_ln_g; ca.tr_ln_b = tr_ln_b;
+  ca.tr_b1 = tr_b1; ca.tr_b2 = tr_b2;
+  ca.o_s = o_s;
+  layers_kernel<<<384, 128, 0, stream>>>(ca, sync_cnt);
+
+  gemm_kernel<3, 0, 1, 0, 0, 0, 0><<<dim3(2, 32), 128, 0, stream>>>(
       s_cur, nullptr, nullptr, nullptr,
       ps_arwin, ps_arwin + 49152, ps_arwin + 98304,
       ar_bin, abuf, nullptr, nullptr, 1024, 128, 384);
-  gemm_kernel<3, 0, 1, 0, 1, 0, 0><<<dim3(4, 32), 128, 0, stream>>>(
+  gemm_kernel<3, 0, 1, 0, 1, 0, 0><<<dim3(2, 32), 128, 0, stream>>>(
       s_init, nullptr, nullptr, nullptr,
       ps_arwinit, ps_arwinit + 49152, ps_arwinit + 98304,
       ar_binit, abuf, nullptr, nullptr, 1024, 128, 384);
   for (int j = 0; j < 2; ++j) {
-    gemm_kernel<3, 0, 1, 0, 0, 0, 0><<<dim3(4, 32), 128, 0, stream>>>(
+    gemm_kernel<3, 0, 1, 0, 0, 0, 0><<<dim3(2, 32), 128, 0, stream>>>(
         abuf, nullptr, nullptr, nullptr,
         ps_arw1 + j * 16384, ps_arw1 + 32768 + j * 16384, ps_arw1 + 65536 + j * 16384,
         ar_b1 + j * 128, htmp, nullptr, nullptr, 1024, 128, 128);
-    gemm_kernel<3, 0, 1, 0, 1, 0, 0><<<dim3(4, 32), 128, 0, stream>>>(
+    gemm_kernel<3, 0, 1, 0, 1, 0, 0><<<dim3(2, 32), 128, 0, stream>>>(
         htmp, nullptr, nullptr, nullptr,
         ps_arw2 + j * 16384, ps_arw2 + 32768 + j * 16384, ps_arw2 + 65536 + j * 16384,
         ar_b2 + j * 128, abuf, nullptr, nullptr, 1024, 128, 128);
```
